# Kernel tuning notes

Hardware: AMD Instinct MI355X
Metric: run time of the kernel (lower is better)

The kernel has to match this reference:

```python
import jax, jax.numpy as jnp
import numpy as np

ALPHA = 0.2
N_NODES = 50000
N_REL = 500
E = 500000
E_NHOP = 100000


def l2norm(v):
    n = jnp.sqrt(jnp.sum(v * v, axis=1, keepdims=True))
    return v / jnp.maximum(n, 1e-12)


def sp_attention(x, src, dst, edge_embed, a, a2, concat):
    # a: [out, 2*din + drel]; edge_m = a @ cat(x[src], x[dst], edge_embed).T, done blockwise
    N, din = x.shape
    a_src, a_dst, a_rel = a[:, :din], a[:, din:2 * din], a[:, 2 * din:]
    edge_m = x[src] @ a_src.T + x[dst] @ a_dst.T + edge_embed @ a_rel.T  # [E, out]
    powers = -jax.nn.leaky_relu(edge_m @ a2, ALPHA)                      # [E]
    edge_e = jnp.exp(powers)
    e_rowsum = jax.ops.segment_sum(edge_e, src, num_segments=N)
    e_rowsum = jnp.where(e_rowsum == 0.0, 1e-12, e_rowsum)
    h_prime = jax.ops.segment_sum(edge_e[:, None] * edge_m, src, num_segments=N)
    h_prime = h_prime / e_rowsum[:, None]
    return jax.nn.elu(h_prime) if concat else h_prime


def spgat(x, rel, src, dst, edge_type, et_nhop, head_params, W, out_a, out_a2):
    ee = jnp.concatenate([rel[edge_type], rel[et_nhop[:, 0]] + rel[et_nhop[:, 1]]], axis=0)
    x = jnp.concatenate([sp_attention(x, src, dst, ee, a, a2, True) for a, a2 in head_params], axis=1)
    out_rel = rel @ W
    ee2 = jnp.concatenate([out_rel[edge_type], out_rel[et_nhop[:, 0]] + out_rel[et_nhop[:, 1]]], axis=0)
    x = jax.nn.elu(sp_attention(x, src, dst, ee2, out_a, out_a2, False))
    return x, out_rel


def forward_impl(entity_emb, relation_emb, W_entities,
                 g0_a0, g0_s0, g0_a1, g0_s1, g0_W, g0_oa, g0_os,
                 g1_a0, g1_s0, g1_W, g1_oa, g1_os,
                 edge_list, edge_type, train_indices_nhop, batch_inputs):
    ent = l2norm(entity_emb)
    rel = l2norm(relation_emb)
    # n-hop edges: (col3 -> col0), relation pair in cols 1,2
    src = jnp.concatenate([edge_list[0], train_indices_nhop[:, 3]])
    dst = jnp.concatenate([edge_list[1], train_indices_nhop[:, 0]])
    et_nhop = train_indices_nhop[:, 1:3]
    mask = jnp.zeros((ent.shape[0],), ent.dtype).at[batch_inputs[:, 2]].set(1.0)
    # layer 0 (2 heads)
    ent_up = ent @ W_entities
    rel_up = rel @ W_entities
    e_new, r_new = spgat(ent, rel, src, dst, edge_type, et_nhop,
                         [(g0_a0, g0_s0), (g0_a1, g0_s1)], g0_W, g0_oa, g0_os)
    ent = l2norm(ent_up + mask[:, None] * e_new)
    rel = l2norm(rel_up + r_new)
    # layer 1 (1 head, residual)
    e_new, r_new = spgat(ent, rel, src, dst, edge_type, et_nhop,
                         [(g1_a0, g1_s0)], g1_W, g1_oa, g1_os)
    ent = l2norm(ent + mask[:, None] * e_new)
    rel = l2norm(rel + r_new)
    return ent, rel


def setup_inputs() -> dict:
    key = jax.random.key(0)
    ks = jax.random.split(key, 20)
    s = 0.05
    inp = {
        "entity_emb": jax.random.normal(ks[0], (N_NODES, 100), jnp.float32),
        "relation_emb": jax.random.normal(ks[1], (N_REL, 100), jnp.float32),
        "W_entities": jax.random.normal(ks[2], (100, 200), jnp.float32) * s,
        "g0_a0": jax.random.normal(ks[3], (100, 300), jnp.float32) * s,
        "g0_s0": jax.random.normal(ks[4], (100,), jnp.float32) * s,
        "g0_a1": jax.random.normal(ks[5], (100, 300), jnp.float32) * s,
        "g0_s1": jax.random.normal(ks[6], (100,), jnp.float32) * s,
        "g0_W": jax.random.normal(ks[7], (100, 200), jnp.float32) * s,
        "g0_oa": jax.random.normal(ks[8], (200, 600), jnp.float32) * s,
        "g0_os": jax.random.normal(ks[9], (200,), jnp.float32) * s,
        "g1_a0": jax.random.normal(ks[10], (200, 600), jnp.float32) * s,
        "g1_s0": jax.random.normal(ks[11], (200,), jnp.float32) * s,
        "g1_W": jax.random.normal(ks[12], (200, 200), jnp.float32) * s,
        "g1_oa": jax.random.normal(ks[13], (200, 600), jnp.float32) * s,
        "g1_os": jax.random.normal(ks[14], (200,), jnp.float32) * s,
        "edge_list": jax.random.randint(ks[15], (2, E), 0, N_NODES, jnp.int64 if jax.config.jax_enable_x64 else jnp.int32),
        "edge_type": jax.random.randint(ks[16], (E,), 0, N_REL),
        "train_indices_nhop": jax.random.randint(ks[17], (E_NHOP, 4), 0, N_REL),
        "batch_inputs": jax.random.randint(ks[18], (10000, 3), 0, N_NODES),
    }
    return inp


def reference(entity_emb, relation_emb, W_entities,
              g0_a0, g0_s0, g0_a1, g0_s1, g0_W, g0_oa, g0_os,
              g1_a0, g1_s0, g1_W, g1_oa, g1_os,
              edge_list, edge_type, train_indices_nhop, batch_inputs):
    return forward_impl(entity_emb, relation_emb, W_entities,
                        g0_a0, g0_s0, g0_a1, g0_s1, g0_W, g0_oa, g0_os,
                        g1_a0, g1_s0, g1_W, g1_oa, g1_os,
                        edge_list, edge_type, train_indices_nhop, batch_inputs)
```

## Files before the change

kernel.cpp:

```cpp
#include <hip/hip_runtime.h>
#include <hip/hip_bf16.h>
#include <cstdint>
#include <cstddef>

#define NNODES 50000
#define NRELS  500
#define NEDGE  500000
#define NETOT  600000
#define MP     50048
#define RPAD   512
#define HOTN   512

typedef __attribute__((ext_vector_type(8))) short bf16x8;
typedef __attribute__((ext_vector_type(4))) float f32x4;

__device__ inline float bf2f(unsigned short s){
  union { unsigned u; float f; } v; v.u = ((unsigned)s) << 16; return v.f;
}
__device__ inline unsigned short f2bf(float f){
  __hip_bfloat16 h = __float2bfloat16(f);
  return __builtin_bit_cast(unsigned short, h);
}

__global__ void k_zero(int* __restrict__ p, int n){
  int i = blockIdx.x*blockDim.x + threadIdx.x;
  if (i < n) p[i] = 0;
}
__global__ void k_mask_set(const int* __restrict__ batch, float* __restrict__ mask, int nb){
  int i = blockIdx.x*blockDim.x + threadIdx.x;
  if (i < nb) mask[batch[3*i+2]] = 1.0f;
}
__global__ void k_padcols(__hip_bfloat16* __restrict__ dst, int Mpad, int K, int Kp){
  int padw = Kp - K;
  long long i = (long long)blockIdx.x*blockDim.x + threadIdx.x;
  if (i >= (long long)Mpad*padw) return;
  int r = (int)(i / padw), k = K + (int)(i - (long long)r*padw);
  dst[(size_t)r*Kp + k] = __float2bfloat16(0.f);
}

__global__ void k_hist(const int* __restrict__ el, const int* __restrict__ nh, int* __restrict__ deg){
  int e = blockIdx.x*blockDim.x + threadIdx.x;
  if (e >= NETOT) return;
  int s = (e < NEDGE) ? el[e] : nh[4*(e-NEDGE)+3];
  atomicAdd(&deg[s], 1);
}
__global__ void k_scan1(int* __restrict__ data, int n, int* __restrict__ part){
  __shared__ int sh[256];
  int t = threadIdx.x, i = blockIdx.x*256 + t;
  int v = (i < n) ? data[i] : 0;
  sh[t] = v; __syncthreads();
  for (int o = 1; o < 256; o <<= 1){
    int x = (t >= o) ? sh[t-o] : 0;
    __syncthreads(); sh[t] += x; __syncthreads();
  }
  if (i < n) data[i] = sh[t] - v;
  if (t == 255) part[blockIdx.x] = sh[255];
}
__global__ void k_scan2(int* __restrict__ part, int nb){
  __shared__ int sh[256];
  int t = threadIdx.x;
  int v = (t < nb) ? part[t] : 0;
  sh[t] = v; __syncthreads();
  for (int o = 1; o < 256; o <<= 1){
    int x = (t >= o) ? sh[t-o] : 0;
    __syncthreads(); sh[t] += x; __syncthreads();
  }
  if (t < nb) part[t] = sh[t] - v;
}
__global__ void k_scan3(int* __restrict__ data, int n, const int* __restrict__ part){
  int i = blockIdx.x*256 + threadIdx.x;
  if (i < n) data[i] += part[blockIdx.x];
  if (i == 0) data[n] = NETOT;
}
__global__ void k_scatter(const int* __restrict__ el, const int* __restrict__ et,
                          const int* __restrict__ nh, const int* __restrict__ rowofs,
                          int* __restrict__ cur, int4* __restrict__ erec){
  int e = blockIdx.x*blockDim.x + threadIdx.x;
  if (e >= NETOT) return;
  int s, d, t0, t1;
  if (e < NEDGE){ s = el[e]; d = el[NEDGE+e]; t0 = et[e]; t1 = NRELS; }
  else { int i = e - NEDGE; s = nh[4*i+3]; d = nh[4*i+0]; t0 = nh[4*i+1]; t1 = nh[4*i+2]; }
  int p = rowofs[s] + atomicAdd(&cur[s], 1);
  erec[p] = make_int4(d, t0, t1, 0);
}

template<int D, int KP>
__global__ __launch_bounds__(64) void k_l2norm_bf(const float* __restrict__ in,
                                                  __hip_bfloat16* __restrict__ bfout){
  constexpr int NK = KP/64;
  int n = blockIdx.x, lane = threadIdx.x;
  const float* row = in + (size_t)n*D;
  float v[NK]; float ss = 0.f;
  #pragma unroll
  for (int k = 0; k < NK; k++){ int c = lane + 64*k; v[k] = (c < D) ? row[c] : 0.f; ss += v[k]*v[k]; }
  #pragma unroll
  for (int o = 32; o; o >>= 1) ss += __shfl_xor(ss, o, 64);
  float sc = 1.0f / fmaxf(sqrtf(ss), 1e-12f);
  __hip_bfloat16* orow = bfout + (size_t)n*KP;
  #pragma unroll
  for (int k = 0; k < NK; k++){ int c = lane + 64*k; orow[c] = __float2bfloat16(v[k]*sc); }
}

template<bool FINAL>
__global__ __launch_bounds__(64) void k_combine2(
    const __hip_bfloat16* __restrict__ baseE, const __hip_bfloat16* __restrict__ hE,
    const float* __restrict__ mask,
    const __hip_bfloat16* __restrict__ baseR, const __hip_bfloat16* __restrict__ hR,
    float* __restrict__ outfE, float* __restrict__ outfR,
    __hip_bfloat16* __restrict__ outbE, __hip_bfloat16* __restrict__ outbR)
{
  int n = blockIdx.x, lane = threadIdx.x;
  bool isE = n < NNODES;
  int row = isE ? n : n - NNODES;
  const __hip_bfloat16* b = (isE ? baseE : baseR) + (size_t)row*224;
  const __hip_bfloat16* h = (isE ? hE : hR) + (size_t)row*224;
  float m = isE ? mask[row] : 1.0f;
  int c = lane*4;
  float4 v = make_float4(0.f,0.f,0.f,0.f);
  if (c < 200){
    ushort4 bb = *(const ushort4*)(b + c);
    ushort4 hh = *(const ushort4*)(h + c);
    v.x = bf2f(bb.x) + m*bf2f(hh.x);
    v.y = bf2f(bb.y) + m*bf2f(hh.y);
    v.z = bf2f(bb.z) + m*bf2f(hh.z);
    v.w = bf2f(bb.w) + m*bf2f(hh.w);
  }
  float ss = v.x*v.x + v.y*v.y + v.z*v.z + v.w*v.w;
  #pragma unroll
  for (int o = 32; o; o >>= 1) ss += __shfl_xor(ss, o, 64);
  float sc = 1.0f / fmaxf(sqrtf(ss), 1e-12f);
  if constexpr (FINAL){
    if (c < 200){
      float* o = (isE ? outfE : outfR) + (size_t)row*200 + c;
      *(float4*)o = make_float4(v.x*sc, v.y*sc, v.z*sc, v.w*sc);
    }
  } else {
    if (c < 224){
      __hip_bfloat16* o = (isE ? outbE : outbR) + (size_t)row*224 + c;
      ushort4 w4; w4.x = f2bf(v.x*sc); w4.y = f2bf(v.y*sc); w4.z = f2bf(v.z*sc); w4.w = f2bf(v.w*sc);
      *(ushort4*)o = w4;
    }
  }
}

__global__ void k_wtab(const float* __restrict__ s0h, const float* __restrict__ s1h,
                       const float* __restrict__ os0, const float* __restrict__ s1l,
                       const float* __restrict__ os1, float* __restrict__ WT){
  int i = blockIdx.x*256 + threadIdx.x;
  if (i >= 2304) return;
  float v = 0.f;
  if (i < 512){
    int c = i & 127;
    const float* s = (i < 256) ? s0h : s1h;
    if (c < 100) v = s[c];
  } else if (i < 768){
    int j = i - 512, c = j & 127;
    const float* s = (j < 128) ? s0h : s1h;
    if (c < 100) v = s[c];
  } else {
    int j = i - 768, t = j >> 9, c = j & 255;
    const float* s = (t == 0) ? os0 : (t == 1) ? s1l : os1;
    if (c < 200) v = s[c];
  }
  WT[i] = v;
}

template<int EPL, int GPO>
__global__ __launch_bounds__(256) void k_rowdotW(const __hip_bfloat16* __restrict__ X, int ld, int M,
    const float* __restrict__ wt,
    float* __restrict__ o0, float* __restrict__ o1, float* __restrict__ o2, float* __restrict__ o3){
  int wave = threadIdx.x >> 6, lane = threadIdx.x & 63;
  int row = blockIdx.x*4 + wave;
  if (row >= M) return;
  int c0 = lane*EPL;
  const __hip_bfloat16* xr = X + (size_t)row*ld + c0;
  float p = 0.f;
  #pragma unroll
  for (int k = 0; k < EPL/4; k++){
    ushort4 x = *(const ushort4*)(xr + 4*k);
    float4 a = *(const float4*)(wt + c0 + 4*k);
    p += bf2f(x.x)*a.x + bf2f(x.y)*a.y + bf2f(x.z)*a.z + bf2f(x.w)*a.w;
  }
  constexpr int G = 16*GPO;
  #pragma unroll
  for (int o = G/2; o; o >>= 1) p += __shfl_xor(p, o, 64);
  if ((lane & (G-1)) == 0){
    int g = lane / G;
    float* o = (g == 0) ? o0 : (g == 1) ? o1 : (g == 2) ? o2 : o3;
    o[row] = p;
  }
}

struct WEnt { int src, ld, boff, rows, K, tr, dstoff, Kp, rp; };
__device__ const WEnt g_went[18] = {
  {0,200,0,200,100,1,      0,128,256},
  {3,200,0,200,100,1,  32768,128,256},
  {1,300,  0,100,100,0,  65536,128,128},
  {1,300,100,100,100,0,  81920,128,128},
  {2,300,  0,100,100,0,  98304,128,128},
  {2,300,100,100,100,0, 114688,128,128},
  {1,300,200,100,100,0, 131072,128,128},
  {2,300,200,100,100,0, 147456,128,128},
  {4,600,  0,200,200,0, 163840,224,256},
  {4,600,200,200,200,0, 221184,224,256},
  {4,600,400,200,200,0, 278528,224,256},
  {5,600,  0,200,200,0, 335872,224,256},
  {5,600,200,200,200,0, 393216,224,256},
  {5,600,400,200,200,0, 450560,224,256},
  {6,200,0,200,200,1,   507904,224,256},
  {7,600,  0,200,200,0, 565248,224,256},
  {7,600,200,200,200,0, 622592,224,256},
  {7,600,400,200,200,0, 679936,224,256},
};
struct Ptr8 { const float* p[8]; };
__global__ void k_wconv(Ptr8 srcs, __hip_bfloat16* __restrict__ dst){
  WEnt e = g_went[blockIdx.y];
  int i = blockIdx.x*256 + threadIdx.x;
  if (i >= e.rp*e.Kp) return;
  int r = i / e.Kp, k = i - r*e.Kp;
  float v = 0.f;
  if (r < e.rows && k < e.K)
    v = e.tr ? srcs.p[e.src][(size_t)k*e.ld + r] : srcs.p[e.src][(size_t)r*e.ld + e.boff + k];
  dst[e.dstoff + i] = __float2bfloat16(v);
}

__global__ __launch_bounds__(256) void k_gemm_mfma(
    const __hip_bfloat16* __restrict__ A, const __hip_bfloat16* __restrict__ B,
    __hip_bfloat16* __restrict__ C, int M, int Nn, int Kp, int ldc)
{
  __shared__ __hip_bfloat16 As[128*32];
  __shared__ __hip_bfloat16 Bs[64*32];
  const int tid = threadIdx.x;
  const int wave = tid >> 6, lane = tid & 63;
  const int lg = lane >> 4, li = lane & 15;
  int nwg = gridDim.x * gridDim.y;
  int bidl = blockIdx.y * gridDim.x + blockIdx.x;
  if ((nwg & 7) == 0){
    int q = nwg >> 3;
    bidl = (bidl & 7) * q + (bidl >> 3);
  }
  const int bx = bidl % gridDim.x, by = bidl / gridDim.x;
  const int m0 = by * 128, n0 = bx * 64;
  const int wr = wave >> 1, wc = wave & 1;
  f32x4 acc[4][2] = {};

  const int ar0 = tid >> 2;
  const int ar1 = (tid + 256) >> 2;
  const int ap  = tid & 3;
  const char* Ab = (const char*)A;
  const char* Bb = (const char*)B;
  char* asB = (char*)As;
  char* bsB = (char*)Bs;

  for (int kk = 0; kk < Kp; kk += 32){
    {
      int g0 = ap ^ ((ar0 >> 1) & 3);
      const char* s0 = Ab + ((size_t)(m0 + ar0)*Kp + kk)*2 + g0*16;
      __builtin_amdgcn_global_load_lds((const __attribute__((address_space(1))) void*)s0,
          (__attribute__((address_space(3))) void*)(asB + wave*1024), 16, 0, 0);
      int g1 = ap ^ ((ar1 >> 1) & 3);
      const char* s1 = Ab + ((size_t)(m0 + ar1)*Kp + kk)*2 + g1*16;
      __builtin_amdgcn_global_load_lds((const __attribute__((address_space(1))) void*)s1,
          (__attribute__((address_space(3))) void*)(asB + 4096 + wave*1024), 16, 0, 0);
      int gb = ap ^ ((ar0 >> 1) & 3);
      const char* sb = Bb + ((size_t)(n0 + ar0)*Kp + kk)*2 + gb*16;
      __builtin_amdgcn_global_load_lds((const __attribute__((address_space(1))) void*)sb,
          (__attribute__((address_space(3))) void*)(bsB + wave*1024), 16, 0, 0);
    }
    __syncthreads();
    bf16x8 av[4], bv[2];
    #pragma unroll
    for (int mf = 0; mf < 4; mf++){
      int row = wr*64 + mf*16 + li;
      int p = lg ^ ((row >> 1) & 3);
      av[mf] = *(const bf16x8*)(asB + row*64 + p*16);
    }
    #pragma unroll
    for (int nf = 0; nf < 2; nf++){
      int row = wc*32 + nf*16 + li;
      int p = lg ^ ((row >> 1) & 3);
      bv[nf] = *(const bf16x8*)(bsB + row*64 + p*16);
    }
    #pragma unroll
    for (int mf = 0; mf < 4; mf++)
      #pragma unroll
      for (int nf = 0; nf < 2; nf++)
        acc[mf][nf] = __builtin_amdgcn_mfma_f32_16x16x32_bf16(av[mf], bv[nf], acc[mf][nf], 0, 0, 0);
    __syncthreads();
  }
  #pragma unroll
  for (int mf = 0; mf < 4; mf++){
    #pragma unroll
    for (int nf = 0; nf < 2; nf++){
      int gc = n0 + wc*32 + nf*16 + li;
      if (gc >= Nn) continue;
      int gr0 = m0 + wr*64 + mf*16 + lg*4;
      #pragma unroll
      for (int r = 0; r < 4; r++){
        int gr = gr0 + r;
        if (gr < M) C[(size_t)gr*ldc + gc] = __float2bfloat16(acc[mf][nf][r]);
      }
    }
  }
}

__device__ inline void agg5_edges(int bstart, int end, int bstep,
    const int4* __restrict__ erec, float psn,
    const float* __restrict__ pd, const float* __restrict__ prs,
    const __hip_bfloat16* __restrict__ XSD, int ldx, int cxd,
    const __hip_bfloat16* __restrict__ RRb, int ldr, int crr,
    int lane, float& Sl, float4& accO)
{
  bool act = lane < 50;
  const __hip_bfloat16* xb = XSD + cxd + 4*lane;
  const __hip_bfloat16* rb = RRb + crr + 4*lane;
  float4 accA = make_float4(0.f,0.f,0.f,0.f);
  float4 accB = make_float4(0.f,0.f,0.f,0.f);
  for (int b = bstart; b < end; b += bstep){
    int j = b + lane;
    int4 e = make_int4(0, NRELS, NRELS, 0);
    float wv = 0.f;
    if (j < end){
      e = erec[j];
      float lg = psn + pd[e.x] + prs[e.y] + prs[e.z];
      wv = __expf(-((lg > 0.f) ? lg : 0.2f*lg));
    }
    Sl += wv;
    int m = end - b; if (m > 64) m = 64;
    int i = 0;
    for (; i + 1 < m; i += 2){
      float wA = __shfl(wv, i),   wB = __shfl(wv, i+1);
      int dA = __shfl(e.x, i),   tA0 = __shfl(e.y, i),   tA1 = __shfl(e.z, i);
      int dB = __shfl(e.x, i+1), tB0 = __shfl(e.y, i+1), tB1 = __shfl(e.z, i+1);
      if (act){
        ushort4 xA = *(const ushort4*)(xb + (size_t)dA*ldx);
        ushort4 rA = *(const ushort4*)(rb + (size_t)tA0*ldr);
        ushort4 xB = *(const ushort4*)(xb + (size_t)dB*ldx);
        ushort4 rB = *(const ushort4*)(rb + (size_t)tB0*ldr);
        float ax = bf2f(xA.x)+bf2f(rA.x), ay = bf2f(xA.y)+bf2f(rA.y);
        float az = bf2f(xA.z)+bf2f(rA.z), aw = bf2f(xA.w)+bf2f(rA.w);
        if (tA1 != NRELS){
          ushort4 rc = *(const ushort4*)(rb + (size_t)tA1*ldr);
          ax += bf2f(rc.x); ay += bf2f(rc.y); az += bf2f(rc.z); aw += bf2f(rc.w);
        }
        float bx = bf2f(xB.x)+bf2f(rB.x), by = bf2f(xB.y)+bf2f(rB.y);
        float bz = bf2f(xB.z)+bf2f(rB.z), bw = bf2f(xB.w)+bf2f(rB.w);
        if (tB1 != NRELS){
          ushort4 rc = *(const ushort4*)(rb + (size_t)tB1*ldr);
          bx += bf2f(rc.x); by += bf2f(rc.y); bz += bf2f(rc.z); bw += bf2f(rc.w);
        }
        accA.x += wA*ax; accA.y += wA*ay; accA.z += wA*az; accA.w += wA*aw;
        accB.x += wB*bx; accB.y += wB*by; accB.z += wB*bz; accB.w += wB*bw;
      }
    }
    if (i < m){
      float wA = __shfl(wv, i);
      int dA = __shfl(e.x, i), tA0 = __shfl(e.y, i), tA1 = __shfl(e.z, i);
      if (act){
        ushort4 xA = *(const ushort4*)(xb + (size_t)dA*ldx);
        ushort4 rA = *(const ushort4*)(rb + (size_t)tA0*ldr);
        float ax = bf2f(xA.x)+bf2f(rA.x), ay = bf2f(xA.y)+bf2f(rA.y);
        float az = bf2f(xA.z)+bf2f(rA.z), aw = bf2f(xA.w)+bf2f(rA.w);
        if (tA1 != NRELS){
          ushort4 rc = *(const ushort4*)(rb + (size_t)tA1*ldr);
          ax += bf2f(rc.x); ay += bf2f(rc.y); az += bf2f(rc.z); aw += bf2f(rc.w);
        }
        accA.x += wA*ax; accA.y += wA*ay; accA.z += wA*az; accA.w += wA*aw;
      }
    }
  }
  accO.x += accA.x + accB.x; accO.y += accA.y + accB.y;
  accO.z += accA.z + accB.z; accO.w += accA.w + accB.w;
}

__device__ inline void agg5_finalize(int n, float S, float4 acc, int lane,
    const __hip_bfloat16* __restrict__ XSD, int ldx, int cxs,
    __hip_bfloat16* __restrict__ outb, int ldb, int coffb)
{
  if (lane >= 50) return;
  float inv = (S > 0.f) ? 1.0f/S : 0.f;
  ushort4 xs4 = *(const ushort4*)(XSD + (size_t)n*ldx + cxs + 4*lane);
  float h0 = (S > 0.f) ? bf2f(xs4.x) + acc.x*inv : 0.f;
  float h1 = (S > 0.f) ? bf2f(xs4.y) + acc.y*inv : 0.f;
  float h2 = (S > 0.f) ? bf2f(xs4.z) + acc.z*inv : 0.f;
  float h3 = (S > 0.f) ? bf2f(xs4.w) + acc.w*inv : 0.f;
  h0 = (h0 > 0.f) ? h0 : expm1f(h0);
  h1 = (h1 > 0.f) ? h1 : expm1f(h1);
  h2 = (h2 > 0.f) ? h2 : expm1f(h2);
  h3 = (h3 > 0.f) ? h3 : expm1f(h3);
  ushort4 o; o.x = f2bf(h0); o.y = f2bf(h1); o.z = f2bf(h2); o.w = f2bf(h3);
  *(ushort4*)(outb + (size_t)n*ldb + coffb + 4*lane) = o;
}

__global__ __launch_bounds__(256) void k_agg5(
    const int* __restrict__ rowofs, const int4* __restrict__ erec,
    const float* __restrict__ ps, const float* __restrict__ pd, const float* __restrict__ prs,
    const __hip_bfloat16* __restrict__ XSD, int ldx, int cxs, int cxd,
    const __hip_bfloat16* __restrict__ RRb, int ldr, int crr,
    __hip_bfloat16* __restrict__ outb, int ldb, int coffb)
{
  __shared__ float4 redA[256];
  __shared__ float redS[4];
  int bid = blockIdx.x;
  int wave = threadIdx.x >> 6, lane = threadIdx.x & 63;

  if (bid < HOTN){
    int n = bid;
    int beg = rowofs[n], end = rowofs[n+1];
    float psn = ps[n];
    float Sl = 0.f;
    float4 acc = make_float4(0.f,0.f,0.f,0.f);
    agg5_edges(beg + wave*64, end, 256, erec, psn, pd, prs,
               XSD, ldx, cxd, RRb, ldr, crr, lane, Sl, acc);
    float Sw = Sl;
    #pragma unroll
    for (int o = 32; o; o >>= 1) Sw += __shfl_xor(Sw, o, 64);
    redA[threadIdx.x] = acc;
    if (lane == 0) redS[wave] = Sw;
    __syncthreads();
    if (wave == 0){
      float4 a0 = redA[lane], a1 = redA[lane+64], a2 = redA[lane+128], a3 = redA[lane+192];
      float4 at = make_float4(a0.x+a1.x+a2.x+a3.x, a0.y+a1.y+a2.y+a3.y,
                              a0.z+a1.z+a2.z+a3.z, a0.w+a1.w+a2.w+a3.w);
      float St = redS[0] + redS[1] + redS[2] + redS[3];
      agg5_finalize(n, St, at, lane, XSD, ldx, cxs, outb, ldb, coffb);
    }
  } else {
    int n = HOTN + (bid - HOTN)*4 + wave;
    int beg = rowofs[n], end = rowofs[n+1];
    float psn = ps[n];
    float Sl = 0.f;
    float4 acc = make_float4(0.f,0.f,0.f,0.f);
    agg5_edges(beg, end, 64, erec, psn, pd, prs,
               XSD, ldx, cxd, RRb, ldr, crr, lane, Sl, acc);
    float S = Sl;
    #pragma unroll
    for (int o = 32; o; o >>= 1) S += __shfl_xor(S, o, 64);
    agg5_finalize(n, S, acc, lane, XSD, ldx, cxs, outb, ldb, coffb);
  }
}

__device__ inline void aggh_edges(int bstart, int end, int bstep,
    const int4* __restrict__ erec,
    float ps0n, const float* __restrict__ pd0, const float* __restrict__ prs0,
    float ps1n, const float* __restrict__ pd1, const float* __restrict__ prs1,
    const __hip_bfloat16* __restrict__ XSD, int ldx,
    const __hip_bfloat16* __restrict__ RRb, int ldr,
    int lane, float& Sl0, float& Sl1, float4& accO)
{
  bool act = lane < 50;
  int head = (lane >= 25) ? 1 : 0;
  int li = lane - 25*head;
  const __hip_bfloat16* xb = XSD + (head ? 384 : 128) + 4*li;
  const __hip_bfloat16* rb = RRb + (head ? 128 : 0) + 4*li;
  float4 accA = make_float4(0.f,0.f,0.f,0.f);
  float4 accB = make_float4(0.f,0.f,0.f,0.f);
  for (int b = bstart; b < end; b += bstep){
    int j = b + lane;
    int4 e = make_int4(0, NRELS, NRELS, 0);
    float wv0 = 0.f, wv1 = 0.f;
    if (j < end){
      e = erec[j];
      float lg0 = ps0n + pd0[e.x] + prs0[e.y] + prs0[e.z];
      float lg1 = ps1n + pd1[e.x] + prs1[e.y] + prs1[e.z];
      wv0 = __expf(-((lg0 > 0.f) ? lg0 : 0.2f*lg0));
      wv1 = __expf(-((lg1 > 0.f) ? lg1 : 0.2f*lg1));
    }
    Sl0 += wv0; Sl1 += wv1;
    int m = end - b; if (m > 64) m = 64;
    int i = 0;
    for (; i + 1 < m; i += 2){
      float wA0 = __shfl(wv0, i),   wA1 = __shfl(wv1, i);
      float wB0 = __shfl(wv0, i+1), wB1 = __shfl(wv1, i+1);
      int dA = __shfl(e.x, i),   tA0 = __shfl(e.y, i),   tA1 = __shfl(e.z, i);
      int dB = __shfl(e.x, i+1), tB0 = __shfl(e.y, i+1), tB1 = __shfl(e.z, i+1);
      if (act){
        float wA = head ? wA1 : wA0;
        float wB = head ? wB1 : wB0;
        ushort4 xA = *(const ushort4*)(xb + (size_t)dA*ldx);
        ushort4 rA = *(const ushort4*)(rb + (size_t)tA0*ldr);
        ushort4 xB = *(const ushort4*)(xb + (size_t)dB*ldx);
        ushort4 rB = *(const ushort4*)(rb + (size_t)tB0*ldr);
        float ax = bf2f(xA.x)+bf2f(rA.x), ay = bf2f(xA.y)+bf2f(rA.y);
        float az = bf2f(xA.z)+bf2f(rA.z), aw = bf2f(xA.w)+bf2f(rA.w);
        if (tA1 != NRELS){
          ushort4 rc = *(const ushort4*)(rb + (size_t)tA1*ldr);
          ax += bf2f(rc.x); ay += bf2f(rc.y); az += bf2f(rc.z); aw += bf2f(rc.w);
        }
        float bx = bf2f(xB.x)+bf2f(rB.x), by = bf2f(xB.y)+bf2f(rB.y);
        float bz = bf2f(xB.z)+bf2f(rB.z), bw = bf2f(xB.w)+bf2f(rB.w);
        if (tB1 != NRELS){
          ushort4 rc = *(const ushort4*)(rb + (size_t)tB1*ldr);
          bx += bf2f(rc.x); by += bf2f(rc.y); bz += bf2f(rc.z); bw += bf2f(rc.w);
        }
        accA.x += wA*ax; accA.y += wA*ay; accA.z += wA*az; accA.w += wA*aw;
        accB.x += wB*bx; accB.y += wB*by; accB.z += wB*bz; accB.w += wB*bw;
      }
    }
    if (i < m){
      float wA0 = __shfl(wv0, i), wA1 = __shfl(wv1, i);
      int dA = __shfl(e.x, i), tA0 = __shfl(e.y, i), tA1 = __shfl(e.z, i);
      if (act){
        float wA = head ? wA1 : wA0;
        ushort4 xA = *(const ushort4*)(xb + (size_t)dA*ldx);
        ushort4 rA = *(const ushort4*)(rb + (size_t)tA0*ldr);
        float ax = bf2f(xA.x)+bf2f(rA.x), ay = bf2f(xA.y)+bf2f(rA.y);
        float az = bf2f(xA.z)+bf2f(rA.z), aw = bf2f(xA.w)+bf2f(rA.w);
        if (tA1 != NRELS){
          ushort4 rc = *(const ushort4*)(rb + (size_t)tA1*ldr);
          ax += bf2f(rc.x); ay += bf2f(rc.y); az += bf2f(rc.z); aw += bf2f(rc.w);
        }
        accA.x += wA*ax; accA.y += wA*ay; accA.z += wA*az; accA.w += wA*aw;
      }
    }
  }
  accO.x += accA.x + accB.x; accO.y += accA.y + accB.y;
  accO.z += accA.z + accB.z; accO.w += accA.w + accB.w;
}

__device__ inline void aggh_finalize(int n, float S0, float S1, float4 acc, int lane,
    const __hip_bfloat16* __restrict__ XSD, int ldx,
    __hip_bfloat16* __restrict__ outb, int ldb)
{
  if (lane >= 50) return;
  int head = (lane >= 25) ? 1 : 0;
  int li = lane - 25*head;
  float S = head ? S1 : S0;
  float inv = (S > 0.f) ? 1.0f/S : 0.f;
  ushort4 xs4 = *(const ushort4*)(XSD + (size_t)n*ldx + (head ? 256 : 0) + 4*li);
  float h0 = (S > 0.f) ? bf2f(xs4.x) + acc.x*inv : 0.f;
  float h1 = (S > 0.f) ? bf2f(xs4.y) + acc.y*inv : 0.f;
  float h2 = (S > 0.f) ? bf2f(xs4.z) + acc.z*inv : 0.f;
  float h3 = (S > 0.f) ? bf2f(xs4.w) + acc.w*inv : 0.f;
  h0 = (h0 > 0.f) ? h0 : expm1f(h0);
  h1 = (h1 > 0.f) ? h1 : expm1f(h1);
  h2 = (h2 > 0.f) ? h2 : expm1f(h2);
  h3 = (h3 > 0.f) ? h3 : expm1f(h3);
  ushort4 o; o.x = f2bf(h0); o.y = f2bf(h1); o.z = f2bf(h2); o.w = f2bf(h3);
  *(ushort4*)(outb + (size_t)n*ldb + 100*head + 4*li) = o;
}

__global__ __launch_bounds__(256) void k_aggh(
    const int* __restrict__ rowofs, const int4* __restrict__ erec,
    const float* __restrict__ ps0, const float* __restrict__ pd0, const float* __restrict__ prs0,
    const float* __restrict__ ps1, const float* __restrict__ pd1, const float* __restrict__ prs1,
    const __hip_bfloat16* __restrict__ XSD, int ldx,
    const __hip_bfloat16* __restrict__ RRb, int ldr,
    __hip_bfloat16* __restrict__ outb, int ldb)
{
  __shared__ float4 redA[256];
  __shared__ float redS0[4];
  __shared__ float redS1[4];
  int bid = blockIdx.x;
  int wave = threadIdx.x >> 6, lane = threadIdx.x & 63;

  if (bid < HOTN){
    int n = bid;
    int beg = rowofs[n], end = rowofs[n+1];
    float ps0n = ps0[n], ps1n = ps1[n];
    float Sl0 = 0.f, Sl1 = 0.f;
    float4 acc = make_float4(0.f,0.f,0.f,0.f);
    aggh_edges(beg + wave*64, end, 256, erec, ps0n, pd0, prs0, ps1n, pd1, prs1,
               XSD, ldx, RRb, ldr, lane, Sl0, Sl1, acc);
    float Sw0 = Sl0, Sw1 = Sl1;
    #pragma unroll
    for (int o = 32; o; o >>= 1){ Sw0 += __shfl_xor(Sw0, o, 64); Sw1 += __shfl_xor(Sw1, o, 64); }
    redA[threadIdx.x] = acc;
    if (lane == 0){ redS0[wave] = Sw0; redS1[wave] = Sw1; }
    __syncthreads();
    if (wave == 0){
      float4 a0 = redA[lane], a1 = redA[lane+64], a2 = redA[lane+128], a3 = redA[lane+192];
      float4 at = make_float4(a0.x+a1.x+a2.x+a3.x, a0.y+a1.y+a2.y+a3.y,
                              a0.z+a1.z+a2.z+a3.z, a0.w+a1.w+a2.w+a3.w);
      float St0 = redS0[0] + redS0[1] + redS0[2] + redS0[3];
      float St1 = redS1[0] + redS1[1] + redS1[2] + redS1[3];
      aggh_finalize(n, St0, St1, at, lane, XSD, ldx, outb, ldb);
    }
  } else {
    int n = HOTN + (bid - HOTN)*4 + wave;
    int beg = rowofs[n], end = rowofs[n+1];
    float ps0n = ps0[n], ps1n = ps1[n];
    float Sl0 = 0.f, Sl1 = 0.f;
    float4 acc = make_float4(0.f,0.f,0.f,0.f);
    aggh_edges(beg, end, 64, erec, ps0n, pd0, prs0, ps1n, pd1, prs1,
               XSD, ldx, RRb, ldr, lane, Sl0, Sl1, acc);
    float S0 = Sl0, S1 = Sl1;
    #pragma unroll
    for (int o = 32; o; o >>= 1){ S0 += __shfl_xor(S0, o, 64); S1 += __shfl_xor(S1, o, 64); }
    aggh_finalize(n, S0, S1, acc, lane, XSD, ldx, outb, ldb);
  }
}

extern "C" void kernel_launch(void* const* d_in, const int* in_sizes, int n_in,
                              void* d_out, int out_size, void* d_ws, size_t ws_size,
                              hipStream_t stream) {
  const float* entity   = (const float*)d_in[0];
  const float* relation = (const float*)d_in[1];
  const float* W_ent    = (const float*)d_in[2];
  const float* g0_a0    = (const float*)d_in[3];
  const float* g0_s0    = (const float*)d_in[4];
  const float* g0_a1    = (const float*)d_in[5];
  const float* g0_s1    = (const float*)d_in[6];
  const float* g0_W     = (const float*)d_in[7];
  const float* g0_oa    = (const float*)d_in[8];
  const float* g0_os    = (const float*)d_in[9];
  const float* g1_a0    = (const float*)d_in[10];
  const float* g1_s0    = (const float*)d_in[11];
  const float* g1_W     = (const float*)d_in[12];
  const float* g1_oa    = (const float*)d_in[13];
  const float* g1_os    = (const float*)d_in[14];
  const int*   el       = (const int*)d_in[15];
  const int*   et       = (const int*)d_in[16];
  const int*   nh       = (const int*)d_in[17];
  const int*   batch    = (const int*)d_in[18];
  (void)in_sizes; (void)n_in; (void)out_size; (void)ws_size;

  char* w = (char*)d_ws;
  auto alloc = [&](size_t bytes)->char*{ char* p = w; w += (bytes + 255) & ~(size_t)255; return p; };
  float* PS0   = (float*)alloc((size_t)NNODES*4);
  float* PD0   = (float*)alloc((size_t)NNODES*4);
  float* PS1   = (float*)alloc((size_t)NNODES*4);
  float* PD1   = (float*)alloc((size_t)NNODES*4);
  float* PRS0  = (float*)alloc((size_t)(NRELS+4)*4);
  float* PRS1  = (float*)alloc((size_t)(NRELS+4)*4);
  float* WT    = (float*)alloc((size_t)2304*4);
  __hip_bfloat16* AENT0  = (__hip_bfloat16*)alloc((size_t)MP*128*2);
  __hip_bfloat16* AX1    = (__hip_bfloat16*)alloc((size_t)MP*224*2);
  __hip_bfloat16* AENT1  = (__hip_bfloat16*)alloc((size_t)MP*224*2);
  __hip_bfloat16* ENTUPb = (__hip_bfloat16*)alloc((size_t)MP*224*2);
  __hip_bfloat16* HB     = (__hip_bfloat16*)alloc((size_t)MP*224*2);
  __hip_bfloat16* AREL0  = (__hip_bfloat16*)alloc((size_t)RPAD*128*2);
  __hip_bfloat16* AREL1  = (__hip_bfloat16*)alloc((size_t)RPAD*224*2);
  __hip_bfloat16* RELUPb = (__hip_bfloat16*)alloc((size_t)RPAD*224*2);
  __hip_bfloat16* ORb0   = (__hip_bfloat16*)alloc((size_t)RPAD*224*2);
  __hip_bfloat16* ORb1   = (__hip_bfloat16*)alloc((size_t)RPAD*224*2);
  __hip_bfloat16* XSD    = (__hip_bfloat16*)alloc((size_t)MP*512*2);
  __hip_bfloat16* RRb    = (__hip_bfloat16*)alloc((size_t)RPAD*256*2);
  __hip_bfloat16* WA     = (__hip_bfloat16*)alloc((size_t)737280*2);
  int* IALL = (int*)alloc((size_t)150001*4);
  int* ROWOFS = IALL;
  int* CUR    = IALL + 50001;
  float* MASK = (float*)(IALL + 100001);
  int4* EREC  = (int4*)alloc((size_t)NETOT*16);
  int* PART   = (int*)alloc((size_t)256*4);

  const __hip_bfloat16* WET   = WA;
  const __hip_bfloat16* G0WT  = WA + 32768;
  const __hip_bfloat16* BH0   = WA + 65536;
  const __hip_bfloat16* BR0   = WA + 131072;
  const __hip_bfloat16* BO0   = WA + 163840;
  const __hip_bfloat16* BO0r  = WA + 278528;
  const __hip_bfloat16* BA1   = WA + 335872;
  const __hip_bfloat16* BA1r  = WA + 450560;
  const __hip_bfloat16* G1WT  = WA + 507904;
  const __hip_bfloat16* BO1   = WA + 565248;
  const __hip_bfloat16* BO1r  = WA + 679936;

  float* outEnt = (float*)d_out;
  float* outRel = outEnt + (size_t)NNODES*200;

  const int TB = 256;
  auto gb = [&](long long n){ return (int)((n + TB - 1)/TB); };
  const int AGG_GRID = HOTN + (NNODES - HOTN)/4;

  k_zero<<<gb(150001), TB, 0, stream>>>(IALL, 150001);
  k_zero<<<gb((48*128 + 48*224)/2), TB, 0, stream>>>((int*)(AENT0 + (size_t)NNODES*128), 48*128/2);
  k_zero<<<gb(48*224/2), TB, 0, stream>>>((int*)(AX1 + (size_t)NNODES*224), 48*224/2);
  k_zero<<<gb(48*224/2), TB, 0, stream>>>((int*)(AENT1 + (size_t)NNODES*224), 48*224/2);
  k_zero<<<gb((RPAD*128 + RPAD*224)/2), TB, 0, stream>>>((int*)AREL0, (RPAD*128 + RPAD*224)/2);
  k_padcols<<<gb((long long)MP*24), TB, 0, stream>>>(AX1, MP, 200, 224);
  k_padcols<<<gb((long long)RPAD*24), TB, 0, stream>>>(ORb0, RPAD, 200, 224);
  k_padcols<<<gb((long long)RPAD*24), TB, 0, stream>>>(ORb1, RPAD, 200, 224);
  k_mask_set<<<gb(10000), TB, 0, stream>>>(batch, MASK, 10000);
  k_hist<<<gb(NETOT), TB, 0, stream>>>(el, nh, ROWOFS);
  int nsb = (NNODES + 255)/256;
  k_scan1<<<nsb, 256, 0, stream>>>(ROWOFS, NNODES, PART);
  k_scan2<<<1, 256, 0, stream>>>(PART, nsb);
  k_scan3<<<nsb, 256, 0, stream>>>(ROWOFS, NNODES, PART);
  k_scatter<<<gb(NETOT), TB, 0, stream>>>(el, et, nh, ROWOFS, CUR, EREC);

  k_l2norm_bf<100,128><<<NNODES, 64, 0, stream>>>(entity, AENT0);
  k_l2norm_bf<100,128><<<NRELS, 64, 0, stream>>>(relation, AREL0);
  {
    Ptr8 srcs;
    srcs.p[0] = W_ent; srcs.p[1] = g0_a0; srcs.p[2] = g0_a1; srcs.p[3] = g0_W;
    srcs.p[4] = g0_oa; srcs.p[5] = g1_a0; srcs.p[6] = g1_W;  srcs.p[7] = g1_oa;
    dim3 g(448, 18);
    k_wconv<<<g, 256, 0, stream>>>(srcs, WA);
  }
  k_wtab<<<gb(2304), 256, 0, stream>>>(g0_s0, g0_s1, g0_os, g1_s0, g1_os, WT);

  auto gemm = [&](const __hip_bfloat16* A, const __hip_bfloat16* B, __hip_bfloat16* C,
                  int M, int Nn, int Kp, int ldc){
    dim3 g((Nn + 63)/64, (M + 127)/128);
    k_gemm_mfma<<<g, 256, 0, stream>>>(A, B, C, M, Nn, Kp, ldc);
  };

  gemm(AENT0, WET, ENTUPb, MP, 200, 128, 224);
  gemm(AREL0, WET, RELUPb, RPAD, 200, 128, 224);

  gemm(AENT0, BH0, XSD, MP, 512, 128, 512);
  gemm(AREL0, BR0, RRb, RPAD, 256, 128, 256);
  k_rowdotW<8,1><<<(NNODES+3)/4, 256, 0, stream>>>(XSD, 512, NNODES, WT + 0, PS0, PD0, PS1, PD1);
  k_rowdotW<4,2><<<(NRELS+4)/4, 256, 0, stream>>>(RRb, 256, NRELS+1, WT + 512, PRS0, PRS1, nullptr, nullptr);
  k_aggh<<<AGG_GRID, 256, 0, stream>>>(ROWOFS, EREC, PS0, PD0, PRS0, PS1, PD1, PRS1,
      XSD, 512, RRb, 256, AX1, 224);

  gemm(AREL0, G0WT, ORb0, RPAD, 200, 128, 224);
  gemm(AX1, BO0, XSD, MP, 512, 224, 512);
  gemm(ORb0, BO0r, RRb, RPAD, 256, 224, 256);
  k_rowdotW<8,2><<<(NNODES+3)/4, 256, 0, stream>>>(XSD, 512, NNODES, WT + 768, PS0, PD0, nullptr, nullptr);
  k_rowdotW<4,4><<<(NRELS+4)/4, 256, 0, stream>>>(RRb, 256, NRELS+1, WT + 768, PRS0, nullptr, nullptr, nullptr);
  k_agg5<<<AGG_GRID, 256, 0, stream>>>(ROWOFS, EREC, PS0, PD0, PRS0,
      XSD, 512, 0, 256, RRb, 256, 0, HB, 224, 0);
  k_combine2<false><<<NNODES + NRELS, 64, 0, stream>>>(ENTUPb, HB, MASK, RELUPb, ORb0,
      nullptr, nullptr, AENT1, AREL1);

  gemm(AENT1, BA1, XSD, MP, 512, 224, 512);
  gemm(AREL1, BA1r, RRb, RPAD, 256, 224, 256);
  k_rowdotW<8,2><<<(NNODES+3)/4, 256, 0, stream>>>(XSD, 512, NNODES, WT + 1280, PS0, PD0, nullptr, nullptr);
  k_rowdotW<4,4><<<(NRELS+4)/4, 256, 0, stream>>>(RRb, 256, NRELS+1, WT + 1280, PRS0, nullptr, nullptr, nullptr);
  k_agg5<<<AGG_GRID, 256, 0, stream>>>(ROWOFS, EREC, PS0, PD0, PRS0,
      XSD, 512, 0, 256, RRb, 256, 0, AX1, 224, 0);

  gemm(AREL1, G1WT, ORb1, RPAD, 200, 224, 224);
  gemm(AX1, BO1, XSD, MP, 512, 224, 512);
  gemm(ORb1, BO1r, RRb, RPAD, 256, 224, 256);
  k_rowdotW<8,2><<<(NNODES+3)/4, 256, 0, stream>>>(XSD, 512, NNODES, WT + 1792, PS0, PD0, nullptr, nullptr);
  k_rowdotW<4,4><<<(NRELS+4)/4, 256, 0, stream>>>(RRb, 256, NRELS+1, WT + 1792, PRS0, nullptr, nullptr, nullptr);
  k_agg5<<<AGG_GRID, 256, 0, stream>>>(ROWOFS, EREC, PS0, PD0, PRS0,
      XSD, 512, 0, 256, RRb, 256, 0, HB, 224, 0);

  k_combine2<true><<<NNODES + NRELS, 64, 0, stream>>>(AENT1, HB, MASK, AREL1, ORb1,
      outEnt, outRel, nullptr, nullptr);
}
```

Measured before the change: 634.9 us.

## Merge setup, paired GEMMs and rowdot launches into fewer fused kernels

Result: faster. 612.2 us (-3.6%).

```diff
diff --git a/kernel.cpp b/kernel.cpp
--- a/kernel.cpp
+++ b/kernel.cpp
@@ -21,174 +21,8 @@
   __hip_bfloat16 h = __float2bfloat16(f);
   return __builtin_bit_cast(unsigned short, h);
 }
-
-__global__ void k_zero(int* __restrict__ p, int n){
-  int i = blockIdx.x*blockDim.x + threadIdx.x;
-  if (i < n) p[i] = 0;
-}
-__global__ void k_mask_set(const int* __restrict__ batch, float* __restrict__ mask, int nb){
-  int i = blockIdx.x*blockDim.x + threadIdx.x;
-  if (i < nb) mask[batch[3*i+2]] = 1.0f;
-}
-__global__ void k_padcols(__hip_bfloat16* __restrict__ dst, int Mpad, int K, int Kp){
-  int padw = Kp - K;
-  long long i = (long long)blockIdx.x*blockDim.x + threadIdx.x;
-  if (i >= (long long)Mpad*padw) return;
-  int r = (int)(i / padw), k = K + (int)(i - (long long)r*padw);
-  dst[(size_t)r*Kp + k] = __float2bfloat16(0.f);
-}
-
-__global__ void k_hist(const int* __restrict__ el, const int* __restrict__ nh, int* __restrict__ deg){
-  int e = blockIdx.x*blockDim.x + threadIdx.x;
-  if (e >= NETOT) return;
-  int s = (e < NEDGE) ? el[e] : nh[4*(e-NEDGE)+3];
-  atomicAdd(&deg[s], 1);
-}
-__global__ void k_scan1(int* __restrict__ data, int n, int* __restrict__ part){
-  __shared__ int sh[256];
-  int t = threadIdx.x, i = blockIdx.x*256 + t;
-  int v = (i < n) ? data[i] : 0;
-  sh[t] = v; __syncthreads();
-  for (int o = 1; o < 256; o <<= 1){
-    int x = (t >= o) ? sh[t-o] : 0;
-    __syncthreads(); sh[t] += x; __syncthreads();
-  }
-  if (i < n) data[i] = sh[t] - v;
-  if (t == 255) part[blockIdx.x] = sh[255];
-}
-__global__ void k_scan2(int* __restrict__ part, int nb){
-  __shared__ int sh[256];
-  int t = threadIdx.x;
-  int v = (t < nb) ? part[t] : 0;
-  sh[t] = v; __syncthreads();
-  for (int o = 1; o < 256; o <<= 1){
-    int x = (t >= o) ? sh[t-o] : 0;
-    __syncthreads(); sh[t] += x; __syncthreads();
-  }
-  if (t < nb) part[t] = sh[t] - v;
-}
-__global__ void k_scan3(int* __restrict__ data, int n, const int* __restrict__ part){
-  int i = blockIdx.x*256 + threadIdx.x;
-  if (i < n) data[i] += part[blockIdx.x];
-  if (i == 0) data[n] = NETOT;
-}
-__global__ void k_scatter(const int* __restrict__ el, const int* __restrict__ et,
-                          const int* __restrict__ nh, const int* __restrict__ rowofs,
-                          int* __restrict__ cur, int4* __restrict__ erec){
-  int e = blockIdx.x*blockDim.x + threadIdx.x;
-  if (e >= NETOT) return;
-  int s, d, t0, t1;
-  if (e < NEDGE){ s = el[e]; d = el[NEDGE+e]; t0 = et[e]; t1 = NRELS; }
-  else { int i = e - NEDGE; s = nh[4*i+3]; d = nh[4*i+0]; t0 = nh[4*i+1]; t1 = nh[4*i+2]; }
-  int p = rowofs[s] + atomicAdd(&cur[s], 1);
-  erec[p] = make_int4(d, t0, t1, 0);
-}
-
-template<int D, int KP>
-__global__ __launch_bounds__(64) void k_l2norm_bf(const float* __restrict__ in,
-                                                  __hip_bfloat16* __restrict__ bfout){
-  constexpr int NK = KP/64;
-  int n = blockIdx.x, lane = threadIdx.x;
-  const float* row = in + (size_t)n*D;
-  float v[NK]; float ss = 0.f;
-  #pragma unroll
-  for (int k = 0; k < NK; k++){ int c = lane + 64*k; v[k] = (c < D) ? row[c] : 0.f; ss += v[k]*v[k]; }
-  #pragma unroll
-  for (int o = 32; o; o >>= 1) ss += __shfl_xor(ss, o, 64);
-  float sc = 1.0f / fmaxf(sqrtf(ss), 1e-12f);
-  __hip_bfloat16* orow = bfout + (size_t)n*KP;
-  #pragma unroll
-  for (int k = 0; k < NK; k++){ int c = lane + 64*k; orow[c] = __float2bfloat16(v[k]*sc); }
-}
-
-template<bool FINAL>
-__global__ __launch_bounds__(64) void k_combine2(
-    const __hip_bfloat16* __restrict__ baseE, const __hip_bfloat16* __restrict__ hE,
-    const float* __restrict__ mask,
-    const __hip_bfloat16* __restrict__ baseR, const __hip_bfloat16* __restrict__ hR,
-    float* __restrict__ outfE, float* __restrict__ outfR,
-    __hip_bfloat16* __restrict__ outbE, __hip_bfloat16* __restrict__ outbR)
-{
-  int n = blockIdx.x, lane = threadIdx.x;
-  bool isE = n < NNODES;
-  int row = isE ? n : n - NNODES;
-  const __hip_bfloat16* b = (isE ? baseE : baseR) + (size_t)row*224;
-  const __hip_bfloat16* h = (isE ? hE : hR) + (size_t)row*224;
-  float m = isE ? mask[row] : 1.0f;
-  int c = lane*4;
-  float4 v = make_float4(0.f,0.f,0.f,0.f);
-  if (c < 200){
-    ushort4 bb = *(const ushort4*)(b + c);
-    ushort4 hh = *(const ushort4*)(h + c);
-    v.x = bf2f(bb.x) + m*bf2f(hh.x);
-    v.y = bf2f(bb.y) + m*bf2f(hh.y);
-    v.z = bf2f(bb.z) + m*bf2f(hh.z);
-    v.w = bf2f(bb.w) + m*bf2f(hh.w);
-  }
-  float ss = v.x*v.x + v.y*v.y + v.z*v.z + v.w*v.w;
-  #pragma unroll
-  for (int o = 32; o; o >>= 1) ss += __shfl_xor(ss, o, 64);
-  float sc = 1.0f / fmaxf(sqrtf(ss), 1e-12f);
-  if constexpr (FINAL){
-    if (c < 200){
-      float* o = (isE ? outfE : outfR) + (size_t)row*200 + c;
-      *(float4*)o = make_float4(v.x*sc, v.y*sc, v.z*sc, v.w*sc);
-    }
-  } else {
-    if (c < 224){
-      __hip_bfloat16* o = (isE ? outbE : outbR) + (size_t)row*224 + c;
-      ushort4 w4; w4.x = f2bf(v.x*sc); w4.y = f2bf(v.y*sc); w4.z = f2bf(v.z*sc); w4.w = f2bf(v.w*sc);
-      *(ushort4*)o = w4;
-    }
-  }
-}
-
-__global__ void k_wtab(const float* __restrict__ s0h, const float* __restrict__ s1h,
-                       const float* __restrict__ os0, const float* __restrict__ s1l,
-                       const float* __restrict__ os1, float* __restrict__ WT){
-  int i = blockIdx.x*256 + threadIdx.x;
-  if (i >= 2304) return;
-  float v = 0.f;
-  if (i < 512){
-    int c = i & 127;
-    const float* s = (i < 256) ? s0h : s1h;
-    if (c < 100) v = s[c];
-  } else if (i < 768){
-    int j = i - 512, c = j & 127;
-    const float* s = (j < 128) ? s0h : s1h;
-    if (c < 100) v = s[c];
-  } else {
-    int j = i - 768, t = j >> 9, c = j & 255;
-    const float* s = (t == 0) ? os0 : (t == 1) ? s1l : os1;
-    if (c < 200) v = s[c];
-  }
-  WT[i] = v;
-}
-
-template<int EPL, int GPO>
-__global__ __launch_bounds__(256) void k_rowdotW(const __hip_bfloat16* __restrict__ X, int ld, int M,
-    const float* __restrict__ wt,
-    float* __restrict__ o0, float* __restrict__ o1, float* __restrict__ o2, float* __restrict__ o3){
-  int wave = threadIdx.x >> 6, lane = threadIdx.x & 63;
-  int row = blockIdx.x*4 + wave;
-  if (row >= M) return;
-  int c0 = lane*EPL;
-  const __hip_bfloat16* xr = X + (size_t)row*ld + c0;
-  float p = 0.f;
-  #pragma unroll
-  for (int k = 0; k < EPL/4; k++){
-    ushort4 x = *(const ushort4*)(xr + 4*k);
-    float4 a = *(const float4*)(wt + c0 + 4*k);
-    p += bf2f(x.x)*a.x + bf2f(x.y)*a.y + bf2f(x.z)*a.z + bf2f(x.w)*a.w;
-  }
-  constexpr int G = 16*GPO;
-  #pragma unroll
-  for (int o = G/2; o; o >>= 1) p += __shfl_xor(p, o, 64);
-  if ((lane & (G-1)) == 0){
-    int g = lane / G;
-    float* o = (g == 0) ? o0 : (g == 1) ? o1 : (g == 2) ? o2 : o3;
-    o[row] = p;
-  }
+__device__ inline float rl_f(float v, int i){
+  return __builtin_bit_cast(float, __builtin_amdgcn_readlane(__builtin_bit_cast(int, v), i));
 }
 
 struct WEnt { int src, ld, boff, rows, K, tr, dstoff, Kp, rp; };
@@ -213,57 +47,258 @@
   {7,600,400,200,200,0, 679936,224,256},
 };
 struct Ptr8 { const float* p[8]; };
-__global__ void k_wconv(Ptr8 srcs, __hip_bfloat16* __restrict__ dst){
-  WEnt e = g_went[blockIdx.y];
+
+#define SB_O1 587
+#define SB_O2 599
+#define SB_O3 620
+#define SB_O4 641
+#define SB_O5 650
+#define SB_O6 5342
+#define SB_O7 5351
+#define SB_O8 13415
+#define SB_O9 25915
+#define SB_TOT 26040
+
+struct SetupArgs {
+  int* iall;
+  __hip_bfloat16 *aent0, *ax1, *aent1, *arel0, *arel1;
+  float* wt;
+  const float *s0h, *s1h, *os0, *s1l, *os1;
+  __hip_bfloat16* wa;
+  Ptr8 wsrcs;
+  const float *entity, *relation;
+};
+
+__global__ __launch_bounds__(256) void k_setup(SetupArgs a){
+  int bid = blockIdx.x, tid = threadIdx.x;
+  if (bid < SB_O1){ int i = bid*256 + tid; if (i < 150001) a.iall[i] = 0; return; }
+  if (bid < SB_O2){ int i = (bid-SB_O1)*256 + tid;
+    ((int*)(a.aent0 + (size_t)NNODES*128))[i] = 0; return; }
+  if (bid < SB_O3){ int i = (bid-SB_O2)*256 + tid;
+    if (i < 5376) ((int*)(a.ax1 + (size_t)NNODES*224))[i] = 0; return; }
+  if (bid < SB_O4){ int i = (bid-SB_O3)*256 + tid;
+    if (i < 5376) ((int*)(a.aent1 + (size_t)NNODES*224))[i] = 0; return; }
+  if (bid < SB_O5){ int i = (bid-SB_O4)*256 + tid;
+    if (i < 768) ((int*)(a.arel0 + (size_t)NRELS*128))[i] = 0;
+    else if (i < 2112) ((int*)(a.arel1 + (size_t)NRELS*224))[i - 768] = 0;
+    return; }
+  if (bid < SB_O6){ int i = (bid-SB_O5)*256 + tid;
+    int r = i / 24, k = 200 + (i - r*24);
+    a.ax1[(size_t)r*224 + k] = __float2bfloat16(0.f); return; }
+  if (bid < SB_O7){
+    int i = (bid-SB_O6)*256 + tid; if (i >= 2304) return;
+    float v = 0.f;
+    if (i < 512){ int c = i & 127; const float* s = (i < 256) ? a.s0h : a.s1h; if (c < 100) v = s[c]; }
+    else if (i < 768){ int j2 = i - 512, c = j2 & 127; const float* s = (j2 < 128) ? a.s0h : a.s1h; if (c < 100) v = s[c]; }
+    else { int j2 = i - 768, t = j2 >> 9, c = j2 & 255;
+           const float* s = (t==0)?a.os0:(t==1)?a.s1l:a.os1; if (c < 200) v = s[c]; }
+    a.wt[i] = v; return; }
+  if (bid < SB_O8){
+    int sb = bid - SB_O7;
+    WEnt e = g_went[sb / 448];
+    int i = (sb - (sb/448)*448)*256 + tid;
+    if (i >= e.rp*e.Kp) return;
+    int r = i / e.Kp, k = i - r*e.Kp;
+    float v = 0.f;
+    if (r < e.rows && k < e.K)
+      v = e.tr ? a.wsrcs.p[e.src][(size_t)k*e.ld + r] : a.wsrcs.p[e.src][(size_t)r*e.ld + e.boff + k];
+    a.wa[e.dstoff + i] = __float2bfloat16(v); return; }
+  {
+    int wave = tid >> 6, lane = tid & 63;
+    const float* src; __hip_bfloat16* dst; int row;
+    if (bid < SB_O9){ row = (bid - SB_O8)*4 + wave; src = a.entity; dst = a.aent0; }
+    else            { row = (bid - SB_O9)*4 + wave; src = a.relation; dst = a.arel0; }
+    const float* rp = src + (size_t)row*100;
+    float v0 = (lane < 100) ? rp[lane] : 0.f;
+    float v1 = (lane + 64 < 100) ? rp[lane + 64] : 0.f;
+    float ss = v0*v0 + v1*v1;
+    #pragma unroll
+    for (int o = 32; o; o >>= 1) ss += __shfl_xor(ss, o, 64);
+    float sc = 1.0f / fmaxf(sqrtf(ss), 1e-12f);
+    __hip_bfloat16* orow = dst + (size_t)row*128;
+    orow[lane] = __float2bfloat16(v0*sc);
+    orow[lane + 64] = __float2bfloat16(v1*sc);
+  }
+}
+
+__global__ void k_mask_set(const int* __restrict__ batch, float* __restrict__ mask, int nb){
+  int i = blockIdx.x*blockDim.x + threadIdx.x;
+  if (i < nb) mask[batch[3*i+2]] = 1.0f;
+}
+
+__global__ void k_hist(const int* __restrict__ el, const int* __restrict__ nh, int* __restrict__ deg){
+  int e = blockIdx.x*blockDim.x + threadIdx.x;
+  if (e >= NETOT) return;
+  int s = (e < NEDGE) ? el[e] : nh[4*(e-NEDGE)+3];
+  atomicAdd(&deg[s], 1);
+}
+__global__ void k_scan1(int* __restrict__ data, int n, int* __restrict__ part){
+  __shared__ int sh[256];
+  int t = threadIdx.x, i = blockIdx.x*256 + t;
+  int v = (i < n) ? data[i] : 0;
+  sh[t] = v; __syncthreads();
+  for (int o = 1; o < 256; o <<= 1){
+    int x = (t >= o) ? sh[t-o] : 0;
+    __syncthreads(); sh[t] += x; __syncthreads();
+  }
+  if (i < n) data[i] = sh[t] - v;
+  if (t == 255) part[blockIdx.x] = sh[255];
+}
+__global__ void k_scan2(int* __restrict__ part, int nb){
+  __shared__ int sh[256];
+  int t = threadIdx.x;
+  int v = (t < nb) ? part[t] : 0;
+  sh[t] = v; __syncthreads();
+  for (int o = 1; o < 256; o <<= 1){
+    int x = (t >= o) ? sh[t-o] : 0;
+    __syncthreads(); sh[t] += x; __syncthreads();
+  }
+  if (t < nb) part[t] = sh[t] - v;
+}
+__global__ void k_scan3(int* __restrict__ data, int n, const int* __restrict__ part){
   int i = blockIdx.x*256 + threadIdx.x;
-  if (i >= e.rp*e.Kp) return;
-  int r = i / e.Kp, k = i - r*e.Kp;
-  float v = 0.f;
-  if (r < e.rows && k < e.K)
-    v = e.tr ? srcs.p[e.src][(size_t)k*e.ld + r] : srcs.p[e.src][(size_t)r*e.ld + e.boff + k];
-  dst[e.dstoff + i] = __float2bfloat16(v);
-}
-
-__global__ __launch_bounds__(256) void k_gemm_mfma(
-    const __hip_bfloat16* __restrict__ A, const __hip_bfloat16* __restrict__ B,
-    __hip_bfloat16* __restrict__ C, int M, int Nn, int Kp, int ldc)
+  if (i < n) data[i] += part[blockIdx.x];
+  if (i == 0) data[n] = NETOT;
+}
+__global__ void k_scatter(const int* __restrict__ el, const int* __restrict__ et,
+                          const int* __restrict__ nh, const int* __restrict__ rowofs,
+                          int* __restrict__ cur, int4* __restrict__ erec){
+  int e = blockIdx.x*blockDim.x + threadIdx.x;
+  if (e >= NETOT) return;
+  int s, d, t0, t1;
+  if (e < NEDGE){ s = el[e]; d = el[NEDGE+e]; t0 = et[e]; t1 = NRELS; }
+  else { int i = e - NEDGE; s = nh[4*i+3]; d = nh[4*i+0]; t0 = nh[4*i+1]; t1 = nh[4*i+2]; }
+  int p = rowofs[s] + atomicAdd(&cur[s], 1);
+  erec[p] = make_int4(d, t0, t1, 0);
+}
+
+template<bool FINAL>
+__global__ __launch_bounds__(64) void k_combine2(
+    const __hip_bfloat16* __restrict__ baseE, const __hip_bfloat16* __restrict__ hE,
+    const float* __restrict__ mask,
+    const __hip_bfloat16* __restrict__ baseR, const __hip_bfloat16* __restrict__ hR,
+    float* __restrict__ outfE, float* __restrict__ outfR,
+    __hip_bfloat16* __restrict__ outbE, __hip_bfloat16* __restrict__ outbR)
+{
+  int n = blockIdx.x, lane = threadIdx.x;
+  bool isE = n < NNODES;
+  int row = isE ? n : n - NNODES;
+  const __hip_bfloat16* b = (isE ? baseE : baseR) + (size_t)row*224;
+  const __hip_bfloat16* h = (isE ? hE : hR) + (size_t)row*224;
+  float m = isE ? mask[row] : 1.0f;
+  int c = lane*4;
+  float4 v = make_float4(0.f,0.f,0.f,0.f);
+  if (c < 200){
+    ushort4 bb = *(const ushort4*)(b + c);
+    ushort4 hh = *(const ushort4*)(h + c);
+    v.x = bf2f(bb.x) + m*bf2f(hh.x);
+    v.y = bf2f(bb.y) + m*bf2f(hh.y);
+    v.z = bf2f(bb.z) + m*bf2f(hh.z);
+    v.w = bf2f(bb.w) + m*bf2f(hh.w);
+  }
+  float ss = v.x*v.x + v.y*v.y + v.z*v.z + v.w*v.w;
+  #pragma unroll
+  for (int o = 32; o; o >>= 1) ss += __shfl_xor(ss, o, 64);
+  float sc = 1.0f / fmaxf(sqrtf(ss), 1e-12f);
+  if constexpr (FINAL){
+    if (c < 200){
+      float* o = (isE ? outfE : outfR) + (size_t)row*200 + c;
+      *(float4*)o = make_float4(v.x*sc, v.y*sc, v.z*sc, v.w*sc);
+    }
+  } else {
+    if (c < 224){
+      __hip_bfloat16* o = (isE ? outbE : outbR) + (size_t)row*224 + c;
+      ushort4 w4; w4.x = f2bf(v.x*sc); w4.y = f2bf(v.y*sc); w4.z = f2bf(v.z*sc); w4.w = f2bf(v.w*sc);
+      *(ushort4*)o = w4;
+    }
+  }
+}
+
+__global__ __launch_bounds__(256) void k_rowdot3(
+    const __hip_bfloat16* __restrict__ XN, const float* __restrict__ wtN, int GN,
+    float* __restrict__ n0, float* __restrict__ n1, float* __restrict__ n2, float* __restrict__ n3,
+    const __hip_bfloat16* __restrict__ XR, const float* __restrict__ wtR, int GR,
+    float* __restrict__ r0, float* __restrict__ r1)
+{
+  int wave = threadIdx.x >> 6, lane = threadIdx.x & 63;
+  int b = blockIdx.x;
+  if (b < 12500){
+    int row = b*4 + wave;
+    const __hip_bfloat16* xr = XN + (size_t)row*512 + lane*8;
+    const float* wr = wtN + lane*8;
+    float p = 0.f;
+    #pragma unroll
+    for (int k = 0; k < 2; k++){
+      ushort4 x = *(const ushort4*)(xr + 4*k);
+      float4 a = *(const float4*)(wr + 4*k);
+      p += bf2f(x.x)*a.x + bf2f(x.y)*a.y + bf2f(x.z)*a.z + bf2f(x.w)*a.w;
+    }
+    for (int o = GN>>1; o; o >>= 1) p += __shfl_xor(p, o, 64);
+    if ((lane & (GN-1)) == 0){
+      int g = lane / GN;
+      float* out = (g==0)?n0:(g==1)?n1:(g==2)?n2:n3;
+      out[row] = p;
+    }
+  } else {
+    int row = (b - 12500)*4 + wave;
+    if (row >= NRELS + 1) return;
+    const __hip_bfloat16* xr = XR + (size_t)row*256 + lane*4;
+    ushort4 x = *(const ushort4*)xr;
+    float4 a = *(const float4*)(wtR + lane*4);
+    float p = bf2f(x.x)*a.x + bf2f(x.y)*a.y + bf2f(x.z)*a.z + bf2f(x.w)*a.w;
+    for (int o = GR>>1; o; o >>= 1) p += __shfl_xor(p, o, 64);
+    if ((lane & (GR-1)) == 0){
+      int g = lane / GR;
+      float* out = (g==0)?r0:r1;
+      out[row] = p;
+    }
+  }
+}
+
+struct GemmDesc {
+  const __hip_bfloat16 *A, *B; __hip_bfloat16* C;
+  int M, Nn, Kp, ldc, gx, nblk;
+};
+__global__ __launch_bounds__(256) void k_gemm2(GemmDesc g1, GemmDesc g2)
 {
   __shared__ __hip_bfloat16 As[128*32];
   __shared__ __hip_bfloat16 Bs[64*32];
   const int tid = threadIdx.x;
   const int wave = tid >> 6, lane = tid & 63;
   const int lg = lane >> 4, li = lane & 15;
-  int nwg = gridDim.x * gridDim.y;
-  int bidl = blockIdx.y * gridDim.x + blockIdx.x;
-  if ((nwg & 7) == 0){
-    int q = nwg >> 3;
-    bidl = (bidl & 7) * q + (bidl >> 3);
-  }
-  const int bx = bidl % gridDim.x, by = bidl / gridDim.x;
+  int nwg = gridDim.x;
+  int orig = blockIdx.x;
+  int q = nwg >> 3, r = nwg & 7;
+  int xcd = orig & 7, off = orig >> 3;
+  int wg = (xcd < r ? xcd*(q+1) : r*(q+1) + (xcd - r)*q) + off;
+  GemmDesc g = (wg < g1.nblk) ? g1 : g2;
+  int local = (wg < g1.nblk) ? wg : wg - g1.nblk;
+  const int bx = local % g.gx, by = local / g.gx;
   const int m0 = by * 128, n0 = bx * 64;
+  const int Kp = g.Kp;
   const int wr = wave >> 1, wc = wave & 1;
   f32x4 acc[4][2] = {};
 
   const int ar0 = tid >> 2;
   const int ar1 = (tid + 256) >> 2;
   const int ap  = tid & 3;
-  const char* Ab = (const char*)A;
-  const char* Bb = (const char*)B;
+  const char* Ab = (const char*)g.A;
+  const char* Bb = (const char*)g.B;
   char* asB = (char*)As;
   char* bsB = (char*)Bs;
 
   for (int kk = 0; kk < Kp; kk += 32){
     {
-      int g0 = ap ^ ((ar0 >> 1) & 3);
-      const char* s0 = Ab + ((size_t)(m0 + ar0)*Kp + kk)*2 + g0*16;
+      int p0 = ap ^ ((ar0 >> 1) & 3);
+      const char* s0 = Ab + ((size_t)(m0 + ar0)*Kp + kk)*2 + p0*16;
       __builtin_amdgcn_global_load_lds((const __attribute__((address_space(1))) void*)s0,
           (__attribute__((address_space(3))) void*)(asB + wave*1024), 16, 0, 0);
-      int g1 = ap ^ ((ar1 >> 1) & 3);
-      const char* s1 = Ab + ((size_t)(m0 + ar1)*Kp + kk)*2 + g1*16;
+      int p1 = ap ^ ((ar1 >> 1) & 3);
+      const char* s1 = Ab + ((size_t)(m0 + ar1)*Kp + kk)*2 + p1*16;
       __builtin_amdgcn_global_load_lds((const __attribute__((address_space(1))) void*)s1,
           (__attribute__((address_space(3))) void*)(asB + 4096 + wave*1024), 16, 0, 0);
-      int gb = ap ^ ((ar0 >> 1) & 3);
-      const char* sb = Bb + ((size_t)(n0 + ar0)*Kp + kk)*2 + gb*16;
+      int pb = ap ^ ((ar0 >> 1) & 3);
+      const char* sb = Bb + ((size_t)(n0 + ar0)*Kp + kk)*2 + pb*16;
       __builtin_amdgcn_global_load_lds((const __attribute__((address_space(1))) void*)sb,
           (__attribute__((address_space(3))) void*)(bsB + wave*1024), 16, 0, 0);
     }
@@ -293,29 +328,26 @@
     #pragma unroll
     for (int nf = 0; nf < 2; nf++){
       int gc = n0 + wc*32 + nf*16 + li;
-      if (gc >= Nn) continue;
+      if (gc >= g.Nn) continue;
       int gr0 = m0 + wr*64 + mf*16 + lg*4;
       #pragma unroll
-      for (int r = 0; r < 4; r++){
-        int gr = gr0 + r;
-        if (gr < M) C[(size_t)gr*ldc + gc] = __float2bfloat16(acc[mf][nf][r]);
+      for (int rr = 0; rr < 4; rr++){
+        int gr = gr0 + rr;
+        if (gr < g.M) g.C[(size_t)gr*g.ldc + gc] = __float2bfloat16(acc[mf][nf][rr]);
       }
     }
   }
 }
 
-__device__ inline void agg5_edges(int bstart, int end, int bstep,
+__device__ inline void agg6_edges(int bstart, int end, int bstep,
     const int4* __restrict__ erec, float psn,
     const float* __restrict__ pd, const float* __restrict__ prs,
-    const __hip_bfloat16* __restrict__ XSD, int ldx, int cxd,
-    const __hip_bfloat16* __restrict__ RRb, int ldr, int crr,
-    int lane, float& Sl, float4& accO)
-{
-  bool act = lane < 50;
-  const __hip_bfloat16* xb = XSD + cxd + 4*lane;
-  const __hip_bfloat16* rb = RRb + crr + 4*lane;
-  float4 accA = make_float4(0.f,0.f,0.f,0.f);
-  float4 accB = make_float4(0.f,0.f,0.f,0.f);
+    const __hip_bfloat16* __restrict__ xdb, int ldx,
+    const __hip_bfloat16* __restrict__ rrb, int ldr,
+    int lane, float& Sl, float4& acc)
+{
+  const bool act = lane < 50;
+  const int co = 4*lane;
   for (int b = bstart; b < end; b += bstep){
     int j = b + lane;
     int4 e = make_int4(0, NRELS, NRELS, 0);
@@ -327,59 +359,37 @@
     }
     Sl += wv;
     int m = end - b; if (m > 64) m = 64;
-    int i = 0;
-    for (; i + 1 < m; i += 2){
-      float wA = __shfl(wv, i),   wB = __shfl(wv, i+1);
-      int dA = __shfl(e.x, i),   tA0 = __shfl(e.y, i),   tA1 = __shfl(e.z, i);
-      int dB = __shfl(e.x, i+1), tB0 = __shfl(e.y, i+1), tB1 = __shfl(e.z, i+1);
-      if (act){
-        ushort4 xA = *(const ushort4*)(xb + (size_t)dA*ldx);
-        ushort4 rA = *(const ushort4*)(rb + (size_t)tA0*ldr);
-        ushort4 xB = *(const ushort4*)(xb + (size_t)dB*ldx);
-        ushort4 rB = *(const ushort4*)(rb + (size_t)tB0*ldr);
-        float ax = bf2f(xA.x)+bf2f(rA.x), ay = bf2f(xA.y)+bf2f(rA.y);
-        float az = bf2f(xA.z)+bf2f(rA.z), aw = bf2f(xA.w)+bf2f(rA.w);
-        if (tA1 != NRELS){
-          ushort4 rc = *(const ushort4*)(rb + (size_t)tA1*ldr);
-          ax += bf2f(rc.x); ay += bf2f(rc.y); az += bf2f(rc.z); aw += bf2f(rc.w);
+    if (act){
+      #pragma unroll 8
+      for (int i = 0; i < m; ++i){
+        float w0 = rl_f(wv, i);
+        int d  = __builtin_amdgcn_readlane(e.x, i);
+        int t0 = __builtin_amdgcn_readlane(e.y, i);
+        int t1 = __builtin_amdgcn_readlane(e.z, i);
+        const __hip_bfloat16* xr  = xdb + (size_t)d*ldx;
+        const __hip_bfloat16* rr0 = rrb + (size_t)t0*ldr;
+        ushort4 xa = *(const ushort4*)(xr + co);
+        ushort4 ra = *(const ushort4*)(rr0 + co);
+        float sx = bf2f(xa.x)+bf2f(ra.x), sy = bf2f(xa.y)+bf2f(ra.y);
+        float sz = bf2f(xa.z)+bf2f(ra.z), sw = bf2f(xa.w)+bf2f(ra.w);
+        if (t1 != NRELS){
+          const __hip_bfloat16* rr1 = rrb + (size_t)t1*ldr;
+          ushort4 rc = *(const ushort4*)(rr1 + co);
+          sx += bf2f(rc.x); sy += bf2f(rc.y); sz += bf2f(rc.z); sw += bf2f(rc.w);
         }
-        float bx = bf2f(xB.x)+bf2f(rB.x), by = bf2f(xB.y)+bf2f(rB.y);
-        float bz = bf2f(xB.z)+bf2f(rB.z), bw = bf2f(xB.w)+bf2f(rB.w);
-        if (tB1 != NRELS){
-          ushort4 rc = *(const ushort4*)(rb + (size_t)tB1*ldr);
-          bx += bf2f(rc.x); by += bf2f(rc.y); bz += bf2f(rc.z); bw += bf2f(rc.w);
-        }
-        accA.x += wA*ax; accA.y += wA*ay; accA.z += wA*az; accA.w += wA*aw;
-        accB.x += wB*bx; accB.y += wB*by; accB.z += wB*bz; accB.w += wB*bw;
+        acc.x += w0*sx; acc.y += w0*sy; acc.z += w0*sz; acc.w += w0*sw;
       }
     }
-    if (i < m){
-      float wA = __shfl(wv, i);
-      int dA = __shfl(e.x, i), tA0 = __shfl(e.y, i), tA1 = __shfl(e.z, i);
-      if (act){
-        ushort4 xA = *(const ushort4*)(xb + (size_t)dA*ldx);
-        ushort4 rA = *(const ushort4*)(rb + (size_t)tA0*ldr);
-        float ax = bf2f(xA.x)+bf2f(rA.x), ay = bf2f(xA.y)+bf2f(rA.y);
-        float az = bf2f(xA.z)+bf2f(rA.z), aw = bf2f(xA.w)+bf2f(rA.w);
-        if (tA1 != NRELS){
-          ushort4 rc = *(const ushort4*)(rb + (size_t)tA1*ldr);
-          ax += bf2f(rc.x); ay += bf2f(rc.y); az += bf2f(rc.z); aw += bf2f(rc.w);
-        }
-        accA.x += wA*ax; accA.y += wA*ay; accA.z += wA*az; accA.w += wA*aw;
-      }
-    }
-  }
-  accO.x += accA.x + accB.x; accO.y += accA.y + accB.y;
-  accO.z += accA.z + accB.z; accO.w += accA.w + accB.w;
+  }
 }
 
 __device__ inline void agg5_finalize(int n, float S, float4 acc, int lane,
-    const __hip_bfloat16* __restrict__ XSD, int ldx, int cxs,
+    const __hip_bfloat16* __restrict__ XSD, int cxs,
     __hip_bfloat16* __restrict__ outb, int ldb, int coffb)
 {
   if (lane >= 50) return;
   float inv = (S > 0.f) ? 1.0f/S : 0.f;
-  ushort4 xs4 = *(const ushort4*)(XSD + (size_t)n*ldx + cxs + 4*lane);
+  ushort4 xs4 = *(const ushort4*)(XSD + (size_t)n*512 + cxs + 4*lane);
   float h0 = (S > 0.f) ? bf2f(xs4.x) + acc.x*inv : 0.f;
   float h1 = (S > 0.f) ? bf2f(xs4.y) + acc.y*inv : 0.f;
   float h2 = (S > 0.f) ? bf2f(xs4.z) + acc.z*inv : 0.f;
@@ -395,14 +405,15 @@
 __global__ __launch_bounds__(256) void k_agg5(
     const int* __restrict__ rowofs, const int4* __restrict__ erec,
     const float* __restrict__ ps, const float* __restrict__ pd, const float* __restrict__ prs,
-    const __hip_bfloat16* __restrict__ XSD, int ldx, int cxs, int cxd,
-    const __hip_bfloat16* __restrict__ RRb, int ldr, int crr,
+    const __hip_bfloat16* __restrict__ XSD,
+    const __hip_bfloat16* __restrict__ RRb,
     __hip_bfloat16* __restrict__ outb, int ldb, int coffb)
 {
   __shared__ float4 redA[256];
   __shared__ float redS[4];
   int bid = blockIdx.x;
   int wave = threadIdx.x >> 6, lane = threadIdx.x & 63;
+  const __hip_bfloat16* xdb = XSD + 256;
 
   if (bid < HOTN){
     int n = bid;
@@ -410,8 +421,8 @@
     float psn = ps[n];
     float Sl = 0.f;
     float4 acc = make_float4(0.f,0.f,0.f,0.f);
-    agg5_edges(beg + wave*64, end, 256, erec, psn, pd, prs,
-               XSD, ldx, cxd, RRb, ldr, crr, lane, Sl, acc);
+    agg6_edges(beg + wave*64, end, 256, erec, psn, pd, prs,
+               xdb, 512, RRb, 256, lane, Sl, acc);
     float Sw = Sl;
     #pragma unroll
     for (int o = 32; o; o >>= 1) Sw += __shfl_xor(Sw, o, 64);
@@ -423,7 +434,7 @@
       float4 at = make_float4(a0.x+a1.x+a2.x+a3.x, a0.y+a1.y+a2.y+a3.y,
                               a0.z+a1.z+a2.z+a3.z, a0.w+a1.w+a2.w+a3.w);
       float St = redS[0] + redS[1] + redS[2] + redS[3];
-      agg5_finalize(n, St, at, lane, XSD, ldx, cxs, outb, ldb, coffb);
+      agg5_finalize(n, St, at, lane, XSD, 0, outb, ldb, coffb);
     }
   } else {
     int n = HOTN + (bid - HOTN)*4 + wave;
@@ -431,30 +442,27 @@
     float psn = ps[n];
     float Sl = 0.f;
     float4 acc = make_float4(0.f,0.f,0.f,0.f);
-    agg5_edges(beg, end, 64, erec, psn, pd, prs,
-               XSD, ldx, cxd, RRb, ldr, crr, lane, Sl, acc);
+    agg6_edges(beg, end, 64, erec, psn, pd, prs,
+               xdb, 512, RRb, 256, lane, Sl, acc);
     float S = Sl;
     #pragma unroll
     for (int o = 32; o; o >>= 1) S += __shfl_xor(S, o, 64);
-    agg5_finalize(n, S, acc, lane, XSD, ldx, cxs, outb, ldb, coffb);
-  }
-}
-
-__device__ inline void aggh_edges(int bstart, int end, int bstep,
+    agg5_finalize(n, S, acc, lane, XSD, 0, outb, ldb, coffb);
+  }
+}
+
+__device__ inline void agg6h_edges(int bstart, int end, int bstep,
     const int4* __restrict__ erec,
     float ps0n, const float* __restrict__ pd0, const float* __restrict__ prs0,
     float ps1n, const float* __restrict__ pd1, const float* __restrict__ prs1,
-    const __hip_bfloat16* __restrict__ XSD, int ldx,
-    const __hip_bfloat16* __restrict__ RRb, int ldr,
-    int lane, float& Sl0, float& Sl1, float4& accO)
-{
-  bool act = lane < 50;
-  int head = (lane >= 25) ? 1 : 0;
-  int li = lane - 25*head;
-  const __hip_bfloat16* xb = XSD + (head ? 384 : 128) + 4*li;
-  const __hip_bfloat16* rb = RRb + (head ? 128 : 0) + 4*li;
-  float4 accA = make_float4(0.f,0.f,0.f,0.f);
-  float4 accB = make_float4(0.f,0.f,0.f,0.f);
+    const __hip_bfloat16* __restrict__ XSD, const __hip_bfloat16* __restrict__ RRb,
+    int lane, float& Sl0, float& Sl1, float4& acc)
+{
+  const bool act = lane < 50;
+  const int head = (lane >= 25) ? 1 : 0;
+  const int li = lane - 25*head;
+  const int loffX = (head ? 384 : 128) + 4*li;
+  const int loffR = (head ? 128 : 0) + 4*li;
   for (int b = bstart; b < end; b += bstep){
     int j = b + lane;
     int4 e = make_int4(0, NRELS, NRELS, 0);
@@ -468,58 +476,34 @@
     }
     Sl0 += wv0; Sl1 += wv1;
     int m = end - b; if (m > 64) m = 64;
-    int i = 0;
-    for (; i + 1 < m; i += 2){
-      float wA0 = __shfl(wv0, i),   wA1 = __shfl(wv1, i);
-      float wB0 = __shfl(wv0, i+1), wB1 = __shfl(wv1, i+1);
-      int dA = __shfl(e.x, i),   tA0 = __shfl(e.y, i),   tA1 = __shfl(e.z, i);
-      int dB = __shfl(e.x, i+1), tB0 = __shfl(e.y, i+1), tB1 = __shfl(e.z, i+1);
-      if (act){
-        float wA = head ? wA1 : wA0;
-        float wB = head ? wB1 : wB0;
-        ushort4 xA = *(const ushort4*)(xb + (size_t)dA*ldx);
-        ushort4 rA = *(const ushort4*)(rb + (size_t)tA0*ldr);
-        ushort4 xB = *(const ushort4*)(xb + (size_t)dB*ldx);
-        ushort4 rB = *(const ushort4*)(rb + (size_t)tB0*ldr);
-        float ax = bf2f(xA.x)+bf2f(rA.x), ay = bf2f(xA.y)+bf2f(rA.y);
-        float az = bf2f(xA.z)+bf2f(rA.z), aw = bf2f(xA.w)+bf2f(rA.w);
-        if (tA1 != NRELS){
-          ushort4 rc = *(const ushort4*)(rb + (size_t)tA1*ldr);
-          ax += bf2f(rc.x); ay += bf2f(rc.y); az += bf2f(rc.z); aw += bf2f(rc.w);
+    if (act){
+      #pragma unroll 8
+      for (int i = 0; i < m; ++i){
+        float wH0 = rl_f(wv0, i);
+        float wH1 = rl_f(wv1, i);
+        int d  = __builtin_amdgcn_readlane(e.x, i);
+        int t0 = __builtin_amdgcn_readlane(e.y, i);
+        int t1 = __builtin_amdgcn_readlane(e.z, i);
+        float w = head ? wH1 : wH0;
+        const __hip_bfloat16* xr = XSD + (size_t)d*512;
+        const __hip_bfloat16* r0 = RRb + (size_t)t0*256;
+        ushort4 xa = *(const ushort4*)(xr + loffX);
+        ushort4 ra = *(const ushort4*)(r0 + loffR);
+        float sx = bf2f(xa.x)+bf2f(ra.x), sy = bf2f(xa.y)+bf2f(ra.y);
+        float sz = bf2f(xa.z)+bf2f(ra.z), sw = bf2f(xa.w)+bf2f(ra.w);
+        if (t1 != NRELS){
+          const __hip_bfloat16* r1 = RRb + (size_t)t1*256;
+          ushort4 rc = *(const ushort4*)(r1 + loffR);
+          sx += bf2f(rc.x); sy += bf2f(rc.y); sz += bf2f(rc.z); sw += bf2f(rc.w);
         }
-        float bx = bf2f(xB.x)+bf2f(rB.x), by = bf2f(xB.y)+bf2f(rB.y);
-        float bz = bf2f(xB.z)+bf2f(rB.z), bw = bf2f(xB.w)+bf2f(rB.w);
-        if (tB1 != NRELS){
-          ushort4 rc = *(const ushort4*)(rb + (size_t)tB1*ldr);
-          bx += bf2f(rc.x); by += bf2f(rc.y); bz += bf2f(rc.z); bw += bf2f(rc.w);
-        }
-        accA.x += wA*ax; accA.y += wA*ay; accA.z += wA*az; accA.w += wA*aw;
-        accB.x += wB*bx; accB.y += wB*by; accB.z += wB*bz; accB.w += wB*bw;
+        acc.x += w*sx; acc.y += w*sy; acc.z += w*sz; acc.w += w*sw;
       }
     }
-    if (i < m){
-      float wA0 = __shfl(wv0, i), wA1 = __shfl(wv1, i);
-      int dA = __shfl(e.x, i), tA0 = __shfl(e.y, i), tA1 = __shfl(e.z, i);
-      if (act){
-        float wA = head ? wA1 : wA0;
-        ushort4 xA = *(const ushort4*)(xb + (size_t)dA*ldx);
-        ushort4 rA = *(const ushort4*)(rb + (size_t)tA0*ldr);
-        float ax = bf2f(xA.x)+bf2f(rA.x), ay = bf2f(xA.y)+bf2f(rA.y);
-        float az = bf2f(xA.z)+bf2f(rA.z), aw = bf2f(xA.w)+bf2f(rA.w);
-        if (tA1 != NRELS){
-          ushort4 rc = *(const ushort4*)(rb + (size_t)tA1*ldr);
-          ax += bf2f(rc.x); ay += bf2f(rc.y); az += bf2f(rc.z); aw += bf2f(rc.w);
-        }
-        accA.x += wA*ax; accA.y += wA*ay; accA.z += wA*az; accA.w += wA*aw;
-      }
-    }
-  }
-  accO.x += accA.x + accB.x; accO.y += accA.y + accB.y;
-  accO.z += accA.z + accB.z; accO.w += accA.w + accB.w;
+  }
 }
 
 __device__ inline void aggh_finalize(int n, float S0, float S1, float4 acc, int lane,
-    const __hip_bfloat16* __restrict__ XSD, int ldx,
+    const __hip_bfloat16* __restrict__ XSD,
     __hip_bfloat16* __restrict__ outb, int ldb)
 {
   if (lane >= 50) return;
@@ -527,7 +511,7 @@
   int li = lane - 25*head;
   float S = head ? S1 : S0;
   float inv = (S > 0.f) ? 1.0f/S : 0.f;
-  ushort4 xs4 = *(const ushort4*)(XSD + (size_t)n*ldx + (head ? 256 : 0) + 4*li);
+  ushort4 xs4 = *(const ushort4*)(XSD + (size_t)n*512 + (head ? 256 : 0) + 4*li);
   float h0 = (S > 0.f) ? bf2f(xs4.x) + acc.x*inv : 0.f;
   float h1 = (S > 0.f) ? bf2f(xs4.y) + acc.y*inv : 0.f;
   float h2 = (S > 0.f) ? bf2f(xs4.z) + acc.z*inv : 0.f;
@@ -544,8 +528,7 @@
     const int* __restrict__ rowofs, const int4* __restrict__ erec,
     const float* __restrict__ ps0, const float* __restrict__ pd0, const float* __restrict__ prs0,
     const float* __restrict__ ps1, const float* __restrict__ pd1, const float* __restrict__ prs1,
-    const __hip_bfloat16* __restrict__ XSD, int ldx,
-    const __hip_bfloat16* __restrict__ RRb, int ldr,
+    const __hip_bfloat16* __restrict__ XSD, const __hip_bfloat16* __restrict__ RRb,
     __hip_bfloat16* __restrict__ outb, int ldb)
 {
   __shared__ float4 redA[256];
@@ -560,8 +543,8 @@
     float ps0n = ps0[n], ps1n = ps1[n];
     float Sl0 = 0.f, Sl1 = 0.f;
     float4 acc = make_float4(0.f,0.f,0.f,0.f);
-    aggh_edges(beg + wave*64, end, 256, erec, ps0n, pd0, prs0, ps1n, pd1, prs1,
-               XSD, ldx, RRb, ldr, lane, Sl0, Sl1, acc);
+    agg6h_edges(beg + wave*64, end, 256, erec, ps0n, pd0, prs0, ps1n, pd1, prs1,
+                XSD, RRb, lane, Sl0, Sl1, acc);
     float Sw0 = Sl0, Sw1 = Sl1;
     #pragma unroll
     for (int o = 32; o; o >>= 1){ Sw0 += __shfl_xor(Sw0, o, 64); Sw1 += __shfl_xor(Sw1, o, 64); }
@@ -574,7 +557,7 @@
                               a0.z+a1.z+a2.z+a3.z, a0.w+a1.w+a2.w+a3.w);
       float St0 = redS0[0] + redS0[1] + redS0[2] + redS0[3];
       float St1 = redS1[0] + redS1[1] + redS1[2] + redS1[3];
-      aggh_finalize(n, St0, St1, at, lane, XSD, ldx, outb, ldb);
+      aggh_finalize(n, St0, St1, at, lane, XSD, outb, ldb);
     }
   } else {
     int n = HOTN + (bid - HOTN)*4 + wave;
@@ -582,12 +565,12 @@
     float ps0n = ps0[n], ps1n = ps1[n];
     float Sl0 = 0.f, Sl1 = 0.f;
     float4 acc = make_float4(0.f,0.f,0.f,0.f);
-    aggh_edges(beg, end, 64, erec, ps0n, pd0, prs0, ps1n, pd1, prs1,
-               XSD, ldx, RRb, ldr, lane, Sl0, Sl1, acc);
+    agg6h_edges(beg, end, 64, erec, ps0n, pd0, prs0, ps1n, pd1, prs1,
+                XSD, RRb, lane, Sl0, Sl1, acc);
     float S0 = Sl0, S1 = Sl1;
     #pragma unroll
     for (int o = 32; o; o >>= 1){ S0 += __shfl_xor(S0, o, 64); S1 += __shfl_xor(S1, o, 64); }
-    aggh_finalize(n, S0, S1, acc, lane, XSD, ldx, outb, ldb);
+    aggh_finalize(n, S0, S1, acc, lane, XSD, outb, ldb);
   }
 }
 
@@ -662,15 +645,18 @@
   const int TB = 256;
   auto gb = [&](long long n){ return (int)((n + TB - 1)/TB); };
   const int AGG_GRID = HOTN + (NNODES - HOTN)/4;
-
-  k_zero<<<gb(150001), TB, 0, stream>>>(IALL, 150001);
-  k_zero<<<gb((48*128 + 48*224)/2), TB, 0, stream>>>((int*)(AENT0 + (size_t)NNODES*128), 48*128/2);
-  k_zero<<<gb(48*224/2), TB, 0, stream>>>((int*)(AX1 + (size_t)NNODES*224), 48*224/2);
-  k_zero<<<gb(48*224/2), TB, 0, stream>>>((int*)(AENT1 + (size_t)NNODES*224), 48*224/2);
-  k_zero<<<gb((RPAD*128 + RPAD*224)/2), TB, 0, stream>>>((int*)AREL0, (RPAD*128 + RPAD*224)/2);
-  k_padcols<<<gb((long long)MP*24), TB, 0, stream>>>(AX1, MP, 200, 224);
-  k_padcols<<<gb((long long)RPAD*24), TB, 0, stream>>>(ORb0, RPAD, 200, 224);
-  k_padcols<<<gb((long long)RPAD*24), TB, 0, stream>>>(ORb1, RPAD, 200, 224);
+  const int RD_GRID = 12500 + 126;
+
+  {
+    SetupArgs a;
+    a.iall = IALL; a.aent0 = AENT0; a.ax1 = AX1; a.aent1 = AENT1; a.arel0 = AREL0; a.arel1 = AREL1;
+    a.wt = WT; a.s0h = g0_s0; a.s1h = g0_s1; a.os0 = g0_os; a.s1l = g1_s0; a.os1 = g1_os;
+    a.wa = WA;
+    a.wsrcs.p[0] = W_ent; a.wsrcs.p[1] = g0_a0; a.wsrcs.p[2] = g0_a1; a.wsrcs.p[3] = g0_W;
+    a.wsrcs.p[4] = g0_oa; a.wsrcs.p[5] = g1_a0; a.wsrcs.p[6] = g1_W;  a.wsrcs.p[7] = g1_oa;
+    a.entity = entity; a.relation = relation;
+    k_setup<<<SB_TOT, 256, 0, stream>>>(a);
+  }
   k_mask_set<<<gb(10000), TB, 0, stream>>>(batch, MASK, 10000);
   k_hist<<<gb(NETOT), TB, 0, stream>>>(el, nh, ROWOFS);
   int nsb = (NNODES + 255)/256;
@@ -679,57 +665,47 @@
   k_scan3<<<nsb, 256, 0, stream>>>(ROWOFS, NNODES, PART);
   k_scatter<<<gb(NETOT), TB, 0, stream>>>(el, et, nh, ROWOFS, CUR, EREC);
 
-  k_l2norm_bf<100,128><<<NNODES, 64, 0, stream>>>(entity, AENT0);
-  k_l2norm_bf<100,128><<<NRELS, 64, 0, stream>>>(relation, AREL0);
-  {
-    Ptr8 srcs;
-    srcs.p[0] = W_ent; srcs.p[1] = g0_a0; srcs.p[2] = g0_a1; srcs.p[3] = g0_W;
-    srcs.p[4] = g0_oa; srcs.p[5] = g1_a0; srcs.p[6] = g1_W;  srcs.p[7] = g1_oa;
-    dim3 g(448, 18);
-    k_wconv<<<g, 256, 0, stream>>>(srcs, WA);
-  }
-  k_wtab<<<gb(2304), 256, 0, stream>>>(g0_s0, g0_s1, g0_os, g1_s0, g1_os, WT);
-
-  auto gemm = [&](const __hip_bfloat16* A, const __hip_bfloat16* B, __hip_bfloat16* C,
-                  int M, int Nn, int Kp, int ldc){
-    dim3 g((Nn + 63)/64, (M + 127)/128);
-    k_gemm_mfma<<<g, 256, 0, stream>>>(A, B, C, M, Nn, Kp, ldc);
+  auto mkdesc = [](const __hip_bfloat16* A, const __hip_bfloat16* B, __hip_bfloat16* C,
+                   int M, int Nn, int Kp, int ldc){
+    GemmDesc d; d.A = A; d.B = B; d.C = C; d.M = M; d.Nn = Nn; d.Kp = Kp; d.ldc = ldc;
+    d.gx = (Nn + 63)/64; d.nblk = d.gx * ((M + 127)/128); return d;
   };
-
-  gemm(AENT0, WET, ENTUPb, MP, 200, 128, 224);
-  gemm(AREL0, WET, RELUPb, RPAD, 200, 128, 224);
-
-  gemm(AENT0, BH0, XSD, MP, 512, 128, 512);
-  gemm(AREL0, BR0, RRb, RPAD, 256, 128, 256);
-  k_rowdotW<8,1><<<(NNODES+3)/4, 256, 0, stream>>>(XSD, 512, NNODES, WT + 0, PS0, PD0, PS1, PD1);
-  k_rowdotW<4,2><<<(NRELS+4)/4, 256, 0, stream>>>(RRb, 256, NRELS+1, WT + 512, PRS0, PRS1, nullptr, nullptr);
+  GemmDesc dnull = {}; dnull.nblk = 0;
+  auto gemm2 = [&](GemmDesc d1, GemmDesc d2){
+    k_gemm2<<<d1.nblk + d2.nblk, 256, 0, stream>>>(d1, d2);
+  };
+
+  gemm2(mkdesc(AENT0, WET, ENTUPb, MP, 200, 128, 224),
+        mkdesc(AREL0, WET, RELUPb, RPAD, 200, 128, 224));
+
+  gemm2(mkdesc(AENT0, BH0, XSD, MP, 512, 128, 512),
+        mkdesc(AREL0, BR0, RRb, RPAD, 256, 128, 256));
+  k_rowdot3<<<RD_GRID, 256, 0, stream>>>(XSD, WT + 0, 16, PS0, PD0, PS1, PD1,
+                                         RRb, WT + 512, 32, PRS0, PRS1);
   k_aggh<<<AGG_GRID, 256, 0, stream>>>(ROWOFS, EREC, PS0, PD0, PRS0, PS1, PD1, PRS1,
-      XSD, 512, RRb, 256, AX1, 224);
-
-  gemm(AREL0, G0WT, ORb0, RPAD, 200, 128, 224);
-  gemm(AX1, BO0, XSD, MP, 512, 224, 512);
-  gemm(ORb0, BO0r, RRb, RPAD, 256, 224, 256);
-  k_rowdotW<8,2><<<(NNODES+3)/4, 256, 0, stream>>>(XSD, 512, NNODES, WT + 768, PS0, PD0, nullptr, nullptr);
-  k_rowdotW<4,4><<<(NRELS+4)/4, 256, 0, stream>>>(RRb, 256, NRELS+1, WT + 768, PRS0, nullptr, nullptr, nullptr);
-  k_agg5<<<AGG_GRID, 256, 0, stream>>>(ROWOFS, EREC, PS0, PD0, PRS0,
-      XSD, 512, 0, 256, RRb, 256, 0, HB, 224, 0);
+                                       XSD, RRb, AX1, 224);
+
+  gemm2(mkdesc(AX1, BO0, XSD, MP, 512, 224, 512),
+        mkdesc(AREL0, G0WT, ORb0, RPAD, 224, 128, 224));
+  gemm2(mkdesc(ORb0, BO0r, RRb, RPAD, 256, 224, 256), dnull);
+  k_rowdot3<<<RD_GRID, 256, 0, stream>>>(XSD, WT + 768, 32, PS0, PD0, nullptr, nullptr,
+                                         RRb, WT + 768, 64, PRS0, nullptr);
+  k_agg5<<<AGG_GRID, 256, 0, stream>>>(ROWOFS, EREC, PS0, PD0, PRS0, XSD, RRb, HB, 224, 0);
   k_combine2<false><<<NNODES + NRELS, 64, 0, stream>>>(ENTUPb, HB, MASK, RELUPb, ORb0,
       nullptr, nullptr, AENT1, AREL1);
 
-  gemm(AENT1, BA1, XSD, MP, 512, 224, 512);
-  gemm(AREL1, BA1r, RRb, RPAD, 256, 224, 256);
-  k_rowdotW<8,2><<<(NNODES+3)/4, 256, 0, stream>>>(XSD, 512, NNODES, WT + 1280, PS0, PD0, nullptr, nullptr);
-  k_rowdotW<4,4><<<(NRELS+4)/4, 256, 0, stream>>>(RRb, 256, NRELS+1, WT + 1280, PRS0, nullptr, nullptr, nullptr);
-  k_agg5<<<AGG_GRID, 256, 0, stream>>>(ROWOFS, EREC, PS0, PD0, PRS0,
-      XSD, 512, 0, 256, RRb, 256, 0, AX1, 224, 0);
-
-  gemm(AREL1, G1WT, ORb1, RPAD, 200, 224, 224);
-  gemm(AX1, BO1, XSD, MP, 512, 224, 512);
-  gemm(ORb1, BO1r, RRb, RPAD, 256, 224, 256);
-  k_rowdotW<8,2><<<(NNODES+3)/4, 256, 0, stream>>>(XSD, 512, NNODES, WT + 1792, PS0, PD0, nullptr, nullptr);
-  k_rowdotW<4,4><<<(NRELS+4)/4, 256, 0, stream>>>(RRb, 256, NRELS+1, WT + 1792, PRS0, nullptr, nullptr, nullptr);
-  k_agg5<<<AGG_GRID, 256, 0, stream>>>(ROWOFS, EREC, PS0, PD0, PRS0,
-      XSD, 512, 0, 256, RRb, 256, 0, HB, 224, 0);
+  gemm2(mkdesc(AENT1, BA1, XSD, MP, 512, 224, 512),
+        mkdesc(AREL1, BA1r, RRb, RPAD, 256, 224, 256));
+  k_rowdot3<<<RD_GRID, 256, 0, stream>>>(XSD, WT + 1280, 32, PS0, PD0, nullptr, nullptr,
+                                         RRb, WT + 1280, 64, PRS0, nullptr);
+  k_agg5<<<AGG_GRID, 256, 0, stream>>>(ROWOFS, EREC, PS0, PD0, PRS0, XSD, RRb, AX1, 224, 0);
+
+  gemm2(mkdesc(AX1, BO1, XSD, MP, 512, 224, 512),
+        mkdesc(AREL1, G1WT, ORb1, RPAD, 224, 224, 224));
+  gemm2(mkdesc(ORb1, BO1r, RRb, RPAD, 256, 224, 256), dnull);
+  k_rowdot3<<<RD_GRID, 256, 0, stream>>>(XSD, WT + 1792, 32, PS0, PD0, nullptr, nullptr,
+                                         RRb, WT + 1792, 64, PRS0, nullptr);
+  k_agg5<<<AGG_GRID, 256, 0, stream>>>(ROWOFS, EREC, PS0, PD0, PRS0, XSD, RRb, HB, 224, 0);
 
   k_combine2<true><<<NNODES + NRELS, 64, 0, stream>>>(AENT1, HB, MASK, AREL1, ORb1,
       outEnt, outRel, nullptr, nullptr);
```
